# Performance work log

Hardware: AMD Instinct MI355X
Metric: run time of the kernel (lower is better)

Reference implementation:

```python
import jax, jax.numpy as jnp
import numpy as np

NB, H = 4, 16
EPS = 1e-5


def _ln(x, w=None, b=None):
    m = jnp.mean(x, -1, keepdims=True)
    v = jnp.var(x, -1, keepdims=True)
    y = (x - m) * jax.lax.rsqrt(v + EPS)
    if w is not None:
        y = y * w
    if b is not None:
        y = y + b
    return y


def _ada_ln(a, s, ln_s_w, w_gamma, w_beta):
    # AF3 Algorithm 26: a <- sigmoid(Lin(LN_nobias(s))) * LN_noaffine(a) + Lin(LN_nobias(s))
    a_n = _ln(a)
    s_n = _ln(s, ln_s_w)
    return jax.nn.sigmoid(s_n @ w_gamma) * a_n + s_n @ w_beta


def setup_inputs():
    key = jax.random.key(0)
    B, S, c_a, c_s, c_z = 1, 1024, 768, 384, 128
    n_hidden = 2 * c_a  # expansion factor n=2
    ks = iter(jax.random.split(key, 40))

    def rn(shape, scale=1.0):
        return scale * jax.random.normal(next(ks), shape, dtype=jnp.float32)

    p = 0.02
    return {
        "a": rn((B, S, c_a)),
        "s": rn((B, S, c_s)),
        "z": rn((B, S, S, c_z)),
        "beta": rn((B, S, S, H)),
        # per-block AttentionPairBias params (stacked over NB blocks)
        "ln_s_w_attn": jnp.ones((NB, c_s)),
        "wg_attn": rn((NB, c_s, c_a), p),
        "wb_attn": rn((NB, c_s, c_a), p),
        "wq": rn((NB, c_a, c_a), p),
        "bq": jnp.zeros((NB, c_a)),
        "wk": rn((NB, c_a, c_a), p),
        "wv": rn((NB, c_a, c_a), p),
        "ln_z_w": jnp.ones((NB, c_z)),
        "ln_z_b": jnp.zeros((NB, c_z)),
        "wpb": rn((NB, c_z, H), p),
        "wgate": rn((NB, c_a, c_a), p),
        "wo": rn((NB, c_a, c_a), p),
        "wsg_attn": rn((NB, c_s, c_a), p),
        "bsg_attn": -2.0 * jnp.ones((NB, c_a)),
        # per-block ConditionedTransitionBlock params
        "ln_s_w_tr": jnp.ones((NB, c_s)),
        "wg_tr": rn((NB, c_s, c_a), p),
        "wb_tr": rn((NB, c_s, c_a), p),
        "w_swish": rn((NB, c_a, n_hidden), p),
        "w_gate2": rn((NB, c_a, n_hidden), p),
        "wsg_tr": rn((NB, c_s, c_a), p),
        "bsg_tr": -2.0 * jnp.ones((NB, c_a)),
        "w_out": rn((NB, n_hidden, c_a), p),
    }


def reference(a, s, z, beta, ln_s_w_attn, wg_attn, wb_attn, wq, bq, wk, wv,
              ln_z_w, ln_z_b, wpb, wgate, wo, wsg_attn, bsg_attn,
              ln_s_w_tr, wg_tr, wb_tr, w_swish, w_gate2, wsg_tr, bsg_tr, w_out):
    B, S, c_a = a.shape
    d = c_a // H
    scale = 1.0 / jnp.sqrt(jnp.float32(d))
    for i in range(NB):
        # --- AttentionPairBias (AF3 Alg 24) ---
        ah = _ada_ln(a, s, ln_s_w_attn[i], wg_attn[i], wb_attn[i])
        q = (ah @ wq[i] + bq[i]).reshape(B, S, H, d)
        k = (ah @ wk[i]).reshape(B, S, H, d)
        v = (ah @ wv[i]).reshape(B, S, H, d)
        zb = _ln(z, ln_z_w[i], ln_z_b[i]) @ wpb[i]  # [B,S,S,H] pair bias
        scores = jnp.einsum('bihd,bjhd->bhij', q, k) * scale \
                 + jnp.transpose(zb + beta, (0, 3, 1, 2))
        attn = jax.nn.softmax(scores, axis=-1)
        o = jnp.einsum('bhij,bjhd->bihd', attn, v)
        g = jax.nn.sigmoid(ah @ wgate[i]).reshape(B, S, H, d)
        att_out = (g * o).reshape(B, S, c_a) @ wo[i]
        b_attn = jax.nn.sigmoid(s @ wsg_attn[i] + bsg_attn[i]) * att_out
        # --- ConditionedTransitionBlock (AF3 Alg 25, SwiGLU) ---
        th = _ada_ln(a, s, ln_s_w_tr[i], wg_tr[i], wb_tr[i])
        hidden = jax.nn.silu(th @ w_swish[i]) * (th @ w_gate2[i])
        tr = jax.nn.sigmoid(s @ wsg_tr[i] + bsg_tr[i]) * (hidden @ w_out[i])
        a = b_attn + tr
    return a
```

## Files before the change

kernel.cpp:

```cpp
#include <hip/hip_runtime.h>
#include <hip/hip_bf16.h>

typedef __hip_bfloat16 bf16;
typedef __attribute__((ext_vector_type(8))) short s8v;
typedef __attribute__((ext_vector_type(4))) float f4v;

constexpr int S = 1024, CA = 768, CS = 384, CZ = 128, NHID = 1536;
constexpr int NBLK = 4, NHEAD = 16, DH = 48;
constexpr float EPS = 1e-5f;

#define DEV static __device__ __forceinline__

DEV float sigmoidf_(float x) { return 1.0f / (1.0f + __expf(-x)); }

DEV f4v mfma16(s8v a, s8v b, f4v c) {
  return __builtin_amdgcn_mfma_f32_16x16x32_bf16(a, b, c, 0, 0, 0);
}

DEV void gld_lds16(const void* g, void* l) {
  __builtin_amdgcn_global_load_lds((const __attribute__((address_space(1))) void*)g,
                                   (__attribute__((address_space(3))) void*)l, 16, 0, 0);
}

union U8 { s8v s; bf16 h[8]; };
union U4 { uint2 u; bf16 h[4]; };

DEV float wred_sum(float v) {
#pragma unroll
  for (int o = 32; o; o >>= 1) v += __shfl_xor(v, o);
  return v;
}

__global__ __launch_bounds__(256) void rowln_s(const float* __restrict__ x,
                                               bf16* __restrict__ s_hat,
                                               bf16* __restrict__ s_bf) {
  constexpr int C = CS, C4 = C / 4;
  __shared__ float red[8];
  const int t = threadIdx.x;
  const size_t row = blockIdx.x;
  float4 v = make_float4(0.f, 0.f, 0.f, 0.f);
  if (t < C4) v = ((const float4*)(x + row * C))[t];
  float sum = v.x + v.y + v.z + v.w;
  float sq = v.x * v.x + v.y * v.y + v.z * v.z + v.w * v.w;
  sum = wred_sum(sum); sq = wred_sum(sq);
  const int wv = t >> 6;
  if ((t & 63) == 0) { red[2 * wv] = sum; red[2 * wv + 1] = sq; }
  __syncthreads();
  sum = red[0] + red[2] + red[4] + red[6];
  sq = red[1] + red[3] + red[5] + red[7];
  const float m = sum / C;
  const float rstd = rsqrtf(sq / C - m * m + EPS);
  if (t < C4) {
    U4 oh, ob_;
    oh.h[0] = __float2bfloat16((v.x - m) * rstd); oh.h[1] = __float2bfloat16((v.y - m) * rstd);
    oh.h[2] = __float2bfloat16((v.z - m) * rstd); oh.h[3] = __float2bfloat16((v.w - m) * rstd);
    ob_.h[0] = __float2bfloat16(v.x); ob_.h[1] = __float2bfloat16(v.y);
    ob_.h[2] = __float2bfloat16(v.z); ob_.h[3] = __float2bfloat16(v.w);
    *(uint2*)(s_hat + row * C + 4 * t) = oh.u;
    *(uint2*)(s_bf + row * C + 4 * t) = ob_.u;
  }
}

__global__ __launch_bounds__(256) void ln_adaln2(const float* __restrict__ a,
                                                 const bf16* __restrict__ ada,
                                                 bf16* __restrict__ ah_attn,
                                                 bf16* __restrict__ ah_tr) {
  __shared__ float red[8];
  const int t = threadIdx.x;
  const size_t row = blockIdx.x;
  float4 v = make_float4(0.f, 0.f, 0.f, 0.f);
  if (t < 192) v = ((const float4*)(a + row * CA))[t];
  float sum = v.x + v.y + v.z + v.w;
  float sq = v.x * v.x + v.y * v.y + v.z * v.z + v.w * v.w;
  sum = wred_sum(sum); sq = wred_sum(sq);
  const int wv = t >> 6;
  if ((t & 63) == 0) { red[2 * wv] = sum; red[2 * wv + 1] = sq; }
  __syncthreads();
  sum = red[0] + red[2] + red[4] + red[6];
  sq = red[1] + red[3] + red[5] + red[7];
  const float m = sum / CA;
  const float rstd = rsqrtf(sq / CA - m * m + EPS);
  if (t < 192) {
    const float an[4] = {(v.x - m) * rstd, (v.y - m) * rstd, (v.z - m) * rstd, (v.w - m) * rstd};
    const bf16* ar = ada + row * 12288 + 4 * t;
    U4 g1, b1, g2, b2, o1, o2;
    g1.u = *(const uint2*)(ar);
    b1.u = *(const uint2*)(ar + 768);
    g2.u = *(const uint2*)(ar + 1536);
    b2.u = *(const uint2*)(ar + 2304);
#pragma unroll
    for (int j = 0; j < 4; ++j) {
      o1.h[j] = __float2bfloat16(sigmoidf_(__bfloat162float(g1.h[j])) * an[j] + __bfloat162float(b1.h[j]));
      o2.h[j] = __float2bfloat16(sigmoidf_(__bfloat162float(g2.h[j])) * an[j] + __bfloat162float(b2.h[j]));
    }
    *(uint2*)(ah_attn + row * CA + 4 * t) = o1.u;
    *(uint2*)(ah_tr + row * CA + 4 * t) = o2.u;
  }
}

__global__ __launch_bounds__(256) void final_adaln(const float* __restrict__ sg,
                                                   const bf16* __restrict__ att,
                                                   const bf16* __restrict__ tr,
                                                   const bf16* __restrict__ ada,
                                                   bf16* __restrict__ ah_attn,
                                                   bf16* __restrict__ ah_tr) {
  __shared__ float red[8];
  const int t = threadIdx.x;
  const size_t row = blockIdx.x;
  float o[4] = {0.f, 0.f, 0.f, 0.f};
  if (t < 192) {
    const float4 sa = *(const float4*)(sg + row * 6144 + 4 * t);
    const float4 st = *(const float4*)(sg + row * 6144 + 768 + 4 * t);
    U4 av, tv;
    av.u = *(const uint2*)(att + row * CA + 4 * t);
    tv.u = *(const uint2*)(tr + row * CA + 4 * t);
    o[0] = sa.x * __bfloat162float(av.h[0]) + st.x * __bfloat162float(tv.h[0]);
    o[1] = sa.y * __bfloat162float(av.h[1]) + st.y * __bfloat162float(tv.h[1]);
    o[2] = sa.z * __bfloat162float(av.h[2]) + st.z * __bfloat162float(tv.h[2]);
    o[3] = sa.w * __bfloat162float(av.h[3]) + st.w * __bfloat162float(tv.h[3]);
  }
  float sum = o[0] + o[1] + o[2] + o[3];
  float sq = o[0] * o[0] + o[1] * o[1] + o[2] * o[2] + o[3] * o[3];
  sum = wred_sum(sum); sq = wred_sum(sq);
  const int wv = t >> 6;
  if ((t & 63) == 0) { red[2 * wv] = sum; red[2 * wv + 1] = sq; }
  __syncthreads();
  sum = red[0] + red[2] + red[4] + red[6];
  sq = red[1] + red[3] + red[5] + red[7];
  const float m = sum / CA;
  const float rstd = rsqrtf(sq / CA - m * m + EPS);
  if (t < 192) {
    const bf16* ar = ada + row * 12288 + 4 * t;
    U4 g1, b1, g2, b2, o1, o2;
    g1.u = *(const uint2*)(ar);
    b1.u = *(const uint2*)(ar + 768);
    g2.u = *(const uint2*)(ar + 1536);
    b2.u = *(const uint2*)(ar + 2304);
#pragma unroll
    for (int j = 0; j < 4; ++j) {
      const float an = (o[j] - m) * rstd;
      o1.h[j] = __float2bfloat16(sigmoidf_(__bfloat162float(g1.h[j])) * an + __bfloat162float(b1.h[j]));
      o2.h[j] = __float2bfloat16(sigmoidf_(__bfloat162float(g2.h[j])) * an + __bfloat162float(b2.h[j]));
    }
    *(uint2*)(ah_attn + row * CA + 4 * t) = o1.u;
    *(uint2*)(ah_tr + row * CA + 4 * t) = o2.u;
  }
}

struct TGroup {
  const float* src[6];
  bf16* dst[6];
  const float* cs[6];
  long dstZ[6];
};

__global__ __launch_bounds__(256) void transpose_grp(TGroup g, int K, int N, int csZ) {
  __shared__ float tile[32][33];
  const int z = blockIdx.z, wsel = z >> 2, blk = z & 3;
  const float* src = g.src[wsel] + (size_t)blk * K * N;
  bf16* dst = g.dst[wsel] + (size_t)blk * g.dstZ[wsel];
  const float* cs = g.cs[wsel];
  const int k0 = blockIdx.y * 32, n0 = blockIdx.x * 32;
  const int tx = threadIdx.x & 31, ty = threadIdx.x >> 5;
#pragma unroll
  for (int q = 0; q < 4; ++q) {
    const int k = k0 + ty + 8 * q;
    float v = src[(size_t)k * N + n0 + tx];
    if (cs) v *= cs[(size_t)blk * csZ + k];
    tile[ty + 8 * q][tx] = v;
  }
  __syncthreads();
#pragma unroll
  for (int q = 0; q < 4; ++q)
    dst[(size_t)(n0 + ty + 8 * q) * K + k0 + tx] = __float2bfloat16(tile[tx][ty + 8 * q]);
}

__global__ __launch_bounds__(256) void prep_all(const float* __restrict__ ln_z_w,
                                                const float* __restrict__ ln_z_b,
                                                const float* __restrict__ wpb,
                                                bf16* __restrict__ W2T,
                                                float* __restrict__ bias2,
                                                const float* __restrict__ bq,
                                                const float* __restrict__ bsg_attn,
                                                const float* __restrict__ bsg_tr,
                                                float* __restrict__ biasQKVG,
                                                float* __restrict__ biasSG) {
  const int blk = blockIdx.x;
  const int t = threadIdx.x;
  if (blk == 48) {
    for (int f = t; f < 64 * CZ; f += 256) {
      const int col = f >> 7, c = f & 127, b = col >> 4, h = col & 15;
      W2T[f] = __float2bfloat16(ln_z_w[b * CZ + c] * wpb[(b * CZ + c) * NHEAD + h]);
    }
    if (t < 64) {
      const int b = t >> 4, h = t & 15;
      float sum = 0.f;
      for (int c = 0; c < CZ; ++c)
        sum += ln_z_b[b * CZ + c] * wpb[(b * CZ + c) * NHEAD + h];
      bias2[t] = sum;
    }
    return;
  }
  const int g = blk * 256 + t;
  if (g < 4 * 3072) {
    const int b = g / 3072, c = g % 3072;
    biasQKVG[g] = (c < 768) ? bq[b * 768 + c] : 0.f;
  }
  if (g < 6144) {
    const int b = g / 1536, c = g % 1536;
    biasSG[g] = (c < 768) ? bsg_attn[b * 768 + c] : bsg_tr[b * 768 + c - 768];
  }
}

__global__ __launch_bounds__(256) void zbias_kernel(const float* __restrict__ z,
                                                    const float* __restrict__ beta,
                                                    const bf16* __restrict__ W2T,
                                                    const float* __restrict__ bias2,
                                                    bf16* __restrict__ bias_all) {
  __shared__ s8v zt8[64 * 16];
  __shared__ s8v w2s[64 * 16];
  __shared__ float betas[64][17];
  __shared__ float bias2s[64];
  __shared__ bf16 obuf[64][72];
  const int t = threadIdx.x;
  const int i = blockIdx.y, j0 = blockIdx.x * 64;
#pragma unroll
  for (int q = 0; q < 4; ++q) {
    const int u = q * 256 + t;
    const int row = u >> 4, sl = u & 15;
    w2s[row * 16 + (sl ^ (row & 7))] = *(const s8v*)(W2T + row * CZ + sl * 8);
  }
  if (t < 64) bias2s[t] = bias2[t];
  {
    const int j = t >> 2, h4 = t & 3;
    const float4 bv = *(const float4*)(beta + ((size_t)i * S + j0 + j) * NHEAD + 4 * h4);
    betas[j][4 * h4 + 0] = bv.x; betas[j][4 * h4 + 1] = bv.y;
    betas[j][4 * h4 + 2] = bv.z; betas[j][4 * h4 + 3] = bv.w;
  }
  {
    const int p = t >> 2, q = t & 3;
    const float* zr = z + ((size_t)i * S + j0 + p) * CZ + q * 32;
    float vals[32];
    float sum = 0.f, sq = 0.f;
#pragma unroll
    for (int k4 = 0; k4 < 8; ++k4) {
      const float4 xv = *(const float4*)(zr + 4 * k4);
      vals[4 * k4 + 0] = xv.x; vals[4 * k4 + 1] = xv.y;
      vals[4 * k4 + 2] = xv.z; vals[4 * k4 + 3] = xv.w;
      sum += xv.x + xv.y + xv.z + xv.w;
      sq += xv.x * xv.x + xv.y * xv.y + xv.z * xv.z + xv.w * xv.w;
    }
    sum += __shfl_xor(sum, 1); sum += __shfl_xor(sum, 2);
    sq += __shfl_xor(sq, 1); sq += __shfl_xor(sq, 2);
    const float m = sum / CZ;
    const float rstd = rsqrtf(sq / CZ - m * m + EPS);
#pragma unroll
    for (int u = 0; u < 4; ++u) {
      U8 pk;
#pragma unroll
      for (int e = 0; e < 8; ++e) pk.h[e] = __float2bfloat16((vals[8 * u + e] - m) * rstd);
      const int cu = 4 * q + u;
      zt8[p * 16 + (cu ^ (p & 7))] = pk.s;
    }
  }
  __syncthreads();
  const int lane = t & 63, wid = t >> 6;
  const int wr = wid >> 1, wc = wid & 1;
  const int ln = lane & 15, lq = lane >> 4;
  f4v acc[2][2] = {};
#pragma unroll
  for (int kk = 0; kk < 4; ++kk) {
    const int sl = (lq + 4 * kk) ^ (ln & 7);
    s8v a[2], b[2];
#pragma unroll
    for (int mi = 0; mi < 2; ++mi) a[mi] = zt8[(32 * wr + 16 * mi + ln) * 16 + sl];
#pragma unroll
    for (int ni = 0; ni < 2; ++ni) b[ni] = w2s[(32 * wc + 16 * ni + ln) * 16 + sl];
#pragma unroll
    for (int mi = 0; mi < 2; ++mi)
#pragma unroll
      for (int ni = 0; ni < 2; ++ni) acc[mi][ni] = mfma16(a[mi], b[ni], acc[mi][ni]);
  }
#pragma unroll
  for (int mi = 0; mi < 2; ++mi)
#pragma unroll
    for (int ni = 0; ni < 2; ++ni) {
      const int col = 32 * wc + 16 * ni + ln;
      const int jb = 32 * wr + 16 * mi + 4 * lq;
      U4 o4;
#pragma unroll
      for (int r = 0; r < 4; ++r)
        o4.h[r] = __float2bfloat16(acc[mi][ni][r] + bias2s[col] + betas[jb + r][col & 15]);
      *(uint2*)&obuf[col][jb] = o4.u;
    }
  __syncthreads();
  {
    const int oc = t >> 2, js = (t & 3) * 16;
    bf16* dp = bias_all + (size_t)oc * S * S + (size_t)i * S + j0 + js;
    *(s8v*)dp = *(const s8v*)&obuf[oc][js];
    *(s8v*)(dp + 8) = *(const s8v*)&obuf[oc][js + 8];
  }
}

struct Gemm2Args {
  const bf16* A0[2]; int lda0[2];
  const bf16* Bt[2];
  const float* bias[2];
  void* C[2];
  int K[2];
  int nb[2];
  int outMode[2];
  int N[2];
  bf16* vT;
};

__global__ __launch_bounds__(256) void gemm2(Gemm2Args ga) {
  const int z = blockIdx.z;
  if ((int)blockIdx.x >= ga.nb[z]) return;
  __shared__ s8v As[1024];
  __shared__ s8v Bs[1024];
  const bf16* A0 = ga.A0[z]; const int lda0 = ga.lda0[z];
  const bf16* Bt = ga.Bt[z];
  const int K = ga.K[z], N = ga.N[z];
  const int t = threadIdx.x;
  const int lane = t & 63, wid = t >> 6;
  const int wr = wid >> 1, wc = wid & 1;
  const int ln = lane & 15, lq = lane >> 4;
  const int m0 = blockIdx.y * 128, n0 = blockIdx.x * 128;
  int rowA[4], colx[4];
#pragma unroll
  for (int q = 0; q < 4; ++q) {
    const int u = q * 256 + t, row = u >> 3, slp = u & 7;
    rowA[q] = row; colx[q] = (slp ^ (row & 7)) * 8;
  }
  f4v acc[4][4] = {};
  for (int ks = 0; ks < K; ks += 64) {
    __syncthreads();
#pragma unroll
    for (int q = 0; q < 4; ++q) {
      gld_lds16(A0 + (size_t)(m0 + rowA[q]) * lda0 + ks + colx[q], &As[q * 256 + wid * 64]);
      gld_lds16(Bt + (size_t)(n0 + rowA[q]) * K + ks + colx[q], &Bs[q * 256 + wid * 64]);
    }
    __syncthreads();
#pragma unroll
    for (int kk = 0; kk < 2; ++kk) {
      const int sl = (lq + 4 * kk) ^ (ln & 7);
      s8v a[4], b[4];
#pragma unroll
      for (int mi = 0; mi < 4; ++mi) a[mi] = As[(64 * wr + 16 * mi + ln) * 8 + sl];
#pragma unroll
      for (int ni = 0; ni < 4; ++ni) b[ni] = Bs[(64 * wc + 16 * ni + ln) * 8 + sl];
#pragma unroll
      for (int mi = 0; mi < 4; ++mi)
#pragma unroll
        for (int ni = 0; ni < 4; ++ni) acc[mi][ni] = mfma16(a[mi], b[ni], acc[mi][ni]);
    }
  }
  const bool vdiv = (ga.vT != nullptr) && (z == 0) && (n0 >= 1536) && (n0 < 2304);
  const int om = ga.outMode[z];
#pragma unroll
  for (int ni = 0; ni < 4; ++ni) {
    const int n = n0 + 64 * wc + 16 * ni + ln;
    const float bv = ga.bias[z] ? ga.bias[z][n] : 0.f;
#pragma unroll
    for (int mi = 0; mi < 4; ++mi) {
      const int mb = m0 + 64 * wr + 16 * mi + 4 * lq;
      if (vdiv) {
        U4 o4;
#pragma unroll
        for (int r = 0; r < 4; ++r) o4.h[r] = __float2bfloat16(acc[mi][ni][r] + bv);
        *(uint2*)(ga.vT + (size_t)(n - 1536) * S + mb) = o4.u;
      } else if (om == 0) {
        bf16* C = (bf16*)ga.C[z];
#pragma unroll
        for (int r = 0; r < 4; ++r)
          C[(size_t)(mb + r) * N + n] = __float2bfloat16(acc[mi][ni][r] + bv);
      } else {
        float* C = (float*)ga.C[z];
#pragma unroll
        for (int r = 0; r < 4; ++r)
          C[(size_t)(mb + r) * N + n] = sigmoidf_(acc[mi][ni][r] + bv);
      }
    }
  }
}

struct GemmPairArgs {
  const bf16* A0[2]; int lda0[2];
  const bf16* A1[2]; int lda1[2];
  const bf16* Bt[2];
  const float* bias[2];
  bf16* C[2];
  int K[2]; int amode[2];
};

DEV s8v combineRT(s8v x, s8v y, int amode) {
  U8 ux, uy, r;
  ux.s = x; uy.s = y;
#pragma unroll
  for (int j = 0; j < 8; ++j) {
    const float fx = __bfloat162float(ux.h[j]);
    const float fy = __bfloat162float(uy.h[j]);
    const float tt = sigmoidf_(fx);
    r.h[j] = __float2bfloat16((amode == 2 ? fx * tt : tt) * fy);
  }
  return r.s;
}

__global__ __launch_bounds__(256) void gemm_pair(GemmPairArgs ga, int N) {
  __shared__ s8v As[128 * 8];
  __shared__ s8v Bs[128 * 8];
  const int z = blockIdx.z;
  const bf16* A0 = ga.A0[z]; const int lda0 = ga.lda0[z];
  const bf16* A1 = ga.A1[z]; const int lda1 = ga.lda1[z];
  const bf16* Bt = ga.Bt[z];
  const float* bias = ga.bias[z];
  bf16* C = ga.C[z];
  const int K = ga.K[z], amode = ga.amode[z];
  const int t = threadIdx.x;
  const int lane = t & 63, wid = t >> 6;
  const int wr = wid >> 1, wc = wid & 1;
  const int ln = lane & 15, lq = lane >> 4;
  const int m0 = blockIdx.y * 128, n0 = blockIdx.x * 128;
  int rowS[4], slS[4], swz[4];
#pragma unroll
  for (int q = 0; q < 4; ++q) {
    const int u = q * 256 + t;
    rowS[q] = u >> 3; slS[q] = u & 7;
    swz[q] = rowS[q] * 8 + (slS[q] ^ (rowS[q] & 7));
  }
  f4v acc[4][4] = {};
  s8v ra[4], ra2[4], rb[4];
#pragma unroll
  for (int q = 0; q < 4; ++q) {
    ra[q] = *(const s8v*)(A0 + (size_t)(m0 + rowS[q]) * lda0 + slS[q] * 8);
    if (amode != 0) ra2[q] = *(const s8v*)(A1 + (size_t)(m0 + rowS[q]) * lda1 + slS[q] * 8);
    rb[q] = *(const s8v*)(Bt + (size_t)(n0 + rowS[q]) * K + slS[q] * 8);
  }
  for (int ks = 0;;) {
    __syncthreads();
#pragma unroll
    for (int q = 0; q < 4; ++q) {
      As[swz[q]] = (amode == 0) ? ra[q] : combineRT(ra[q], ra2[q], amode);
      Bs[swz[q]] = rb[q];
    }
    const int ksn = ks + 64;
    if (ksn < K) {
#pragma unroll
      for (int q = 0; q < 4; ++q) {
        ra[q] = *(const s8v*)(A0 + (size_t)(m0 + rowS[q]) * lda0 + ksn + slS[q] * 8);
        if (amode != 0) ra2[q] = *(const s8v*)(A1 + (size_t)(m0 + rowS[q]) * lda1 + ksn + slS[q] * 8);
        rb[q] = *(const s8v*)(Bt + (size_t)(n0 + rowS[q]) * K + ksn + slS[q] * 8);
      }
    }
    __syncthreads();
#pragma unroll
    for (int kk = 0; kk < 2; ++kk) {
      const int sl = (lq + 4 * kk) ^ (ln & 7);
      s8v a[4], b[4];
#pragma unroll
      for (int mi = 0; mi < 4; ++mi) a[mi] = As[(64 * wr + 16 * mi + ln) * 8 + sl];
#pragma unroll
      for (int ni = 0; ni < 4; ++ni) b[ni] = Bs[(64 * wc + 16 * ni + ln) * 8 + sl];
#pragma unroll
      for (int mi = 0; mi < 4; ++mi)
#pragma unroll
        for (int ni = 0; ni < 4; ++ni) acc[mi][ni] = mfma16(a[mi], b[ni], acc[mi][ni]);
    }
    ks = ksn;
    if (ks >= K) break;
  }
#pragma unroll
  for (int ni = 0; ni < 4; ++ni) {
    const int n = n0 + 64 * wc + 16 * ni + ln;
    const float bv = bias ? bias[n] : 0.f;
#pragma unroll
    for (int mi = 0; mi < 4; ++mi) {
      const int mb = m0 + 64 * wr + 16 * mi + 4 * lq;
#pragma unroll
      for (int r = 0; r < 4; ++r)
        C[(size_t)(mb + r) * N + n] = __float2bfloat16(acc[mi][ni][r] + bv);
    }
  }
}

__global__ __launch_bounds__(256) void flash_attn(const bf16* __restrict__ qkvg,
                                                  const bf16* __restrict__ vT,
                                                  const bf16* __restrict__ bias_all,
                                                  bf16* __restrict__ ob, int blk) {
  __shared__ s8v Qs[64 * 8];
  __shared__ s8v Ks[2][64 * 8];
  __shared__ s8v Vs[2][48 * 8];
  __shared__ s8v Bs[2][64 * 8];
  __shared__ bf16 PwB[4 * 1024];
  __shared__ float facL[4][16];
  __shared__ float linvL[4][16];
  const int t = threadIdx.x;
  const int lane = t & 63, w = t >> 6;
  const int ln = lane & 15, lq = lane >> 4;
  const int h = blockIdx.y, i0 = blockIdx.x * 64;
  const bf16* bp = bias_all + (size_t)(blk * NHEAD + h) * S * S;
  const float scale = 0.14433756729740643f;

#pragma unroll
  for (int uu = 0; uu < 2; ++uu) {
    const int u = t + 256 * uu, row = u >> 3, sl = u & 7;
    s8v qv{};
    if (sl < 6) qv = *(const s8v*)(qkvg + (size_t)(i0 + row) * 3072 + h * DH + sl * 8);
    Qs[row * 8 + (sl ^ (row & 7))] = qv;
  }

  s8v kr[2], br[2], vr0{}, vr1{};
  auto prefetch = [&](int jt) {
    const int j0 = jt * 64;
#pragma unroll
    for (int uu = 0; uu < 2; ++uu) {
      const int u = t + 256 * uu, row = u >> 3, sl = u & 7;
      s8v kv{};
      if (sl < 6) kv = *(const s8v*)(qkvg + (size_t)(j0 + row) * 3072 + 768 + h * DH + sl * 8);
      kr[uu] = kv;
      br[uu] = *(const s8v*)(bp + (size_t)(i0 + row) * S + j0 + sl * 8);
    }
    { const int d = t >> 3, sl = t & 7;
      vr0 = *(const s8v*)(vT + (size_t)(h * DH + d) * S + j0 + sl * 8); }
    if (t < 128) {
      const int u = 256 + t, d = u >> 3, sl = u & 7;
      vr1 = *(const s8v*)(vT + (size_t)(h * DH + d) * S + j0 + sl * 8);
    }
  };
  auto store_tiles = [&](int pb) {
#pragma unroll
    for (int uu = 0; uu < 2; ++uu) {
      const int u = t + 256 * uu, row = u >> 3, sl = u & 7;
      const int ph = row * 8 + (sl ^ (row & 7));
      Ks[pb][ph] = kr[uu];
      Bs[pb][ph] = br[uu];
    }
    { const int d = t >> 3, sl = t & 7;
      Vs[pb][d * 8 + (sl ^ (d & 7))] = vr0; }
    if (t < 128) {
      const int u = 256 + t, d = u >> 3, sl = u & 7;
      Vs[pb][d * 8 + (sl ^ (d & 7))] = vr1;
    }
  };

  float m_run = -3e30f, l_run = 0.f;
  f4v acc_o[3] = {};
  bf16* pw = PwB + w * 1024;

  prefetch(0);
  for (int jt = 0; jt < 16; ++jt) {
    const int pb = jt & 1;
    __syncthreads();
    store_tiles(pb);
    __syncthreads();
    if (jt < 15) prefetch(jt + 1);
    float p[4][4];
    float tmax = -3e30f;
#pragma unroll
    for (int ja = 0; ja < 4; ++ja) {
      f4v accs = {};
#pragma unroll
      for (int ks2 = 0; ks2 < 2; ++ks2) {
        const int sl = (lq + 4 * ks2) ^ (ln & 7);
        const s8v a = Ks[pb][(16 * ja + ln) * 8 + sl];
        const s8v b = Qs[(16 * w + ln) * 8 + sl];
        accs = mfma16(a, b, accs);
      }
      const int jq = 4 * ja + lq;
      const int pu = jq >> 1;
      U4 bv;
      bv.u = *(const uint2*)((const bf16*)(&Bs[pb][0]) +
                             (((16 * w + ln) * 8 + (pu ^ (ln & 7))) * 8 + (jq & 1) * 4));
#pragma unroll
      for (int r = 0; r < 4; ++r) {
        p[ja][r] = accs[r] * scale + __bfloat162float(bv.h[r]);
        tmax = fmaxf(tmax, p[ja][r]);
      }
    }
    tmax = fmaxf(tmax, __shfl_xor(tmax, 16));
    tmax = fmaxf(tmax, __shfl_xor(tmax, 32));
    const float m_new = fmaxf(m_run, tmax);
    const float fac = __expf(m_run - m_new);
    m_run = m_new;
    float psum = 0.f;
#pragma unroll
    for (int ja = 0; ja < 4; ++ja)
#pragma unroll
      for (int r = 0; r < 4; ++r) {
        p[ja][r] = __expf(p[ja][r] - m_new);
        psum += p[ja][r];
      }
    psum += __shfl_xor(psum, 16);
    psum += __shfl_xor(psum, 32);
    l_run = l_run * fac + psum;
    if (lq == 0) facL[w][ln] = fac;
#pragma unroll
    for (int ja = 0; ja < 4; ++ja) {
      const int ju = 4 * ja + lq;
      const int ph = ju ^ ((ln & 7) << 1);
      U4 pk;
#pragma unroll
      for (int r = 0; r < 4; ++r) pk.h[r] = __float2bfloat16(p[ja][r]);
      *(uint2*)(pw + ln * 64 + ph * 4) = pk.u;
    }
    asm volatile("s_waitcnt lgkmcnt(0)" ::: "memory");
    __builtin_amdgcn_sched_barrier(0);
    const float4 fv = *(const float4*)&facL[w][4 * lq];
#pragma unroll
    for (int ni = 0; ni < 3; ++ni) {
      acc_o[ni][0] *= fv.x; acc_o[ni][1] *= fv.y;
      acc_o[ni][2] *= fv.z; acc_o[ni][3] *= fv.w;
    }
#pragma unroll
    for (int ks2 = 0; ks2 < 2; ++ks2) {
      const int pu0 = (2 * lq + 8 * ks2) ^ ((ln & 7) << 1);
      const s8v pa = *(const s8v*)(pw + ln * 64 + pu0 * 4);
      const int slv = (lq + 4 * ks2) ^ (ln & 7);
#pragma unroll
      for (int ni = 0; ni < 3; ++ni) {
        const s8v vb = Vs[pb][(16 * ni + ln) * 8 + slv];
        acc_o[ni] = mfma16(pa, vb, acc_o[ni]);
      }
    }
  }
  if (lq == 0) linvL[w][ln] = 1.0f / l_run;
  asm volatile("s_waitcnt lgkmcnt(0)" ::: "memory");
  __builtin_amdgcn_sched_barrier(0);
  const float4 lv = *(const float4*)&linvL[w][4 * lq];
  const float lvr[4] = {lv.x, lv.y, lv.z, lv.w};
#pragma unroll
  for (int ni = 0; ni < 3; ++ni)
#pragma unroll
    for (int r = 0; r < 4; ++r) {
      const int m = i0 + 16 * w + 4 * lq + r;
      ob[(size_t)m * CA + h * DH + 16 * ni + ln] = __float2bfloat16(acc_o[ni][r] * lvr[r]);
    }
}

__global__ __launch_bounds__(256) void ew_final(const float* __restrict__ sg,
                                                const bf16* __restrict__ att,
                                                const bf16* __restrict__ tr,
                                                float* __restrict__ out) {
  const int i = blockIdx.x * 256 + threadIdx.x;
  const int row = i / 192, col = (i % 192) * 4;
  const float4 sa = *(const float4*)(sg + (size_t)row * 6144 + col);
  const float4 st = *(const float4*)(sg + (size_t)row * 6144 + 768 + col);
  U4 av, tv;
  av.u = *(const uint2*)(att + (size_t)row * CA + col);
  tv.u = *(const uint2*)(tr + (size_t)row * CA + col);
  float4 o;
  o.x = sa.x * __bfloat162float(av.h[0]) + st.x * __bfloat162float(tv.h[0]);
  o.y = sa.y * __bfloat162float(av.h[1]) + st.y * __bfloat162float(tv.h[1]);
  o.z = sa.z * __bfloat162float(av.h[2]) + st.z * __bfloat162float(tv.h[2]);
  o.w = sa.w * __bfloat162float(av.h[3]) + st.w * __bfloat162float(tv.h[3]);
  *(float4*)(out + (size_t)row * CA + col) = o;
}

__global__ void fill_kernel(float* p, int n, float v) {
  const int i = blockIdx.x * 256 + threadIdx.x;
  if (i < n) p[i] = v;
}

extern "C" void kernel_launch(void* const* d_in, const int* in_sizes, int n_in,
                              void* d_out, int out_size, void* d_ws, size_t ws_size,
                              hipStream_t stream) {
  (void)in_sizes; (void)n_in;
  const float* a_in = (const float*)d_in[0];
  const float* s_in = (const float*)d_in[1];
  const float* z_in = (const float*)d_in[2];
  const float* beta = (const float*)d_in[3];
  const float* ln_s_w_attn = (const float*)d_in[4];
  const float* wg_attn = (const float*)d_in[5];
  const float* wb_attn = (const float*)d_in[6];
  const float* wq = (const float*)d_in[7];
  const float* bq = (const float*)d_in[8];
  const float* wk = (const float*)d_in[9];
  const float* wv = (const float*)d_in[10];
  const float* ln_z_w = (const float*)d_in[11];
  const float* ln_z_b = (const float*)d_in[12];
  const float* wpb = (const float*)d_in[13];
  const float* wgate = (const float*)d_in[14];
  const float* wo = (const float*)d_in[15];
  const float* wsg_attn = (const float*)d_in[16];
  const float* bsg_attn = (const float*)d_in[17];
  const float* ln_s_w_tr = (const float*)d_in[18];
  const float* wg_tr = (const float*)d_in[19];
  const float* wb_tr = (const float*)d_in[20];
  const float* w_swish = (const float*)d_in[21];
  const float* w_gate2 = (const float*)d_in[22];
  const float* wsg_tr = (const float*)d_in[23];
  const float* bsg_tr = (const float*)d_in[24];
  const float* w_out = (const float*)d_in[25];

  char* wp = (char*)d_ws;
  size_t used = 0;
  auto alloc = [&](size_t bytes) -> void* {
    void* p = wp + used;
    used += (bytes + 255) & ~(size_t)255;
    return p;
  };
  bf16* bias_all = (bf16*)alloc((size_t)64 * S * S * 2);
  bf16* WT_ada = (bf16*)alloc((size_t)4 * 3072 * 384 * 2);
  bf16* WT_sg = (bf16*)alloc((size_t)4 * 1536 * 384 * 2);
  bf16* WT_qkvg = (bf16*)alloc((size_t)4 * 3072 * 768 * 2);
  bf16* WT_wo = (bf16*)alloc((size_t)4 * 768 * 768 * 2);
  bf16* WT_mlp = (bf16*)alloc((size_t)4 * 3072 * 768 * 2);
  bf16* WT_wout = (bf16*)alloc((size_t)4 * 768 * 1536 * 2);
  float* biasQKVG = (float*)alloc(4 * 3072 * 4);
  float* biasSG = (float*)alloc(6144 * 4);
  bf16* W2T = (bf16*)alloc(64 * 128 * 2);
  float* bias2 = (float*)alloc(64 * 4);
  bf16* ada_all = (bf16*)alloc((size_t)S * 12288 * 2);
  float* sg_all = (float*)alloc((size_t)S * 6144 * 4);
  bf16* s_hat = (bf16*)alloc((size_t)S * CS * 2);
  bf16* s_bf = (bf16*)alloc((size_t)S * CS * 2);
  bf16* ah_attn = (bf16*)alloc((size_t)S * CA * 2);
  bf16* ah_tr = (bf16*)alloc((size_t)S * CA * 2);
  bf16* qkvg = (bf16*)alloc((size_t)S * 3072 * 2);
  bf16* vT = (bf16*)alloc((size_t)CA * S * 2);
  bf16* ob = (bf16*)alloc((size_t)S * CA * 2);
  bf16* att = (bf16*)alloc((size_t)S * CA * 2);
  bf16* swg = (bf16*)alloc((size_t)S * 3072 * 2);
  bf16* trout = (bf16*)alloc((size_t)S * CA * 2);
  if (used > ws_size) {
    fill_kernel<<<(out_size + 255) / 256, 256, 0, stream>>>((float*)d_out, out_size, 12345.0f);
    return;
  }

  const dim3 B256(256);

  prep_all<<<49, B256, 0, stream>>>(ln_z_w, ln_z_b, wpb, W2T, bias2,
                                    bq, bsg_attn, bsg_tr, biasQKVG, biasSG);

  {
    TGroup g{};
    g.src[0] = wg_attn;  g.dst[0] = WT_ada + (size_t)0 * 384;    g.cs[0] = ln_s_w_attn; g.dstZ[0] = 3072 * 384;
    g.src[1] = wb_attn;  g.dst[1] = WT_ada + (size_t)768 * 384;  g.cs[1] = ln_s_w_attn; g.dstZ[1] = 3072 * 384;
    g.src[2] = wg_tr;    g.dst[2] = WT_ada + (size_t)1536 * 384; g.cs[2] = ln_s_w_tr;   g.dstZ[2] = 3072 * 384;
    g.src[3] = wb_tr;    g.dst[3] = WT_ada + (size_t)2304 * 384; g.cs[3] = ln_s_w_tr;   g.dstZ[3] = 3072 * 384;
    g.src[4] = wsg_attn; g.dst[4] = WT_sg + (size_t)0 * 384;     g.cs[4] = nullptr;     g.dstZ[4] = 1536 * 384;
    g.src[5] = wsg_tr;   g.dst[5] = WT_sg + (size_t)768 * 384;   g.cs[5] = nullptr;     g.dstZ[5] = 1536 * 384;
    transpose_grp<<<dim3(24, 12, 24), B256, 0, stream>>>(g, 384, 768, CS);
  }
  {
    TGroup g{};
    g.src[0] = wq;    g.dst[0] = WT_qkvg + (size_t)0 * 768;    g.dstZ[0] = 3072 * 768;
    g.src[1] = wk;    g.dst[1] = WT_qkvg + (size_t)768 * 768;  g.dstZ[1] = 3072 * 768;
    g.src[2] = wv;    g.dst[2] = WT_qkvg + (size_t)1536 * 768; g.dstZ[2] = 3072 * 768;
    g.src[3] = wgate; g.dst[3] = WT_qkvg + (size_t)2304 * 768; g.dstZ[3] = 3072 * 768;
    g.src[4] = wo;    g.dst[4] = WT_wo;                        g.dstZ[4] = 768 * 768;
    transpose_grp<<<dim3(24, 24, 20), B256, 0, stream>>>(g, 768, 768, 0);
  }
  {
    TGroup g{};
    g.src[0] = w_swish; g.dst[0] = WT_mlp + (size_t)0 * 768;    g.dstZ[0] = 3072 * 768;
    g.src[1] = w_gate2; g.dst[1] = WT_mlp + (size_t)1536 * 768; g.dstZ[1] = 3072 * 768;
    transpose_grp<<<dim3(48, 24, 8), B256, 0, stream>>>(g, 768, 1536, 0);
  }
  {
    TGroup g{};
    g.src[0] = w_out; g.dst[0] = WT_wout; g.dstZ[0] = 768 * 1536;
    transpose_grp<<<dim3(24, 48, 4), B256, 0, stream>>>(g, 1536, 768, 0);
  }

  rowln_s<<<S, B256, 0, stream>>>(s_in, s_hat, s_bf);
  zbias_kernel<<<dim3(16, 1024), B256, 0, stream>>>(z_in, beta, W2T, bias2, bias_all);

  {
    Gemm2Args ga{};
    ga.A0[0] = s_hat; ga.lda0[0] = 384; ga.Bt[0] = WT_ada; ga.bias[0] = nullptr;
    ga.C[0] = ada_all; ga.K[0] = 384; ga.nb[0] = 96; ga.outMode[0] = 0; ga.N[0] = 12288;
    ga.A0[1] = s_bf; ga.lda0[1] = 384; ga.Bt[1] = WT_sg; ga.bias[1] = biasSG;
    ga.C[1] = sg_all; ga.K[1] = 384; ga.nb[1] = 48; ga.outMode[1] = 1; ga.N[1] = 6144;
    ga.vT = nullptr;
    gemm2<<<dim3(96, 8, 2), B256, 0, stream>>>(ga);
  }

  ln_adaln2<<<S, B256, 0, stream>>>(a_in, ada_all, ah_attn, ah_tr);
  for (int b = 0; b < NBLK; ++b) {
    {
      Gemm2Args ga{};
      ga.A0[0] = ah_attn; ga.lda0[0] = 768; ga.Bt[0] = WT_qkvg + (size_t)b * 3072 * 768;
      ga.bias[0] = biasQKVG + b * 3072; ga.C[0] = qkvg; ga.K[0] = 768; ga.nb[0] = 24;
      ga.outMode[0] = 0; ga.N[0] = 3072;
      ga.A0[1] = ah_tr; ga.lda0[1] = 768; ga.Bt[1] = WT_mlp + (size_t)b * 3072 * 768;
      ga.bias[1] = nullptr; ga.C[1] = swg; ga.K[1] = 768; ga.nb[1] = 24;
      ga.outMode[1] = 0; ga.N[1] = 3072;
      ga.vT = vT;
      gemm2<<<dim3(24, 8, 2), B256, 0, stream>>>(ga);
    }
    flash_attn<<<dim3(16, 16), B256, 0, stream>>>(qkvg, vT, bias_all, ob, b);
    {
      GemmPairArgs ga{};
      ga.A0[0] = qkvg + 2304; ga.lda0[0] = 3072; ga.A1[0] = ob; ga.lda1[0] = 768;
      ga.Bt[0] = WT_wo + (size_t)b * 768 * 768; ga.bias[0] = nullptr;
      ga.C[0] = att; ga.K[0] = 768; ga.amode[0] = 1;
      ga.A0[1] = swg; ga.lda0[1] = 3072; ga.A1[1] = swg + 1536; ga.lda1[1] = 3072;
      ga.Bt[1] = WT_wout + (size_t)b * 768 * 1536; ga.bias[1] = nullptr;
      ga.C[1] = trout; ga.K[1] = 1536; ga.amode[1] = 2;
      gemm_pair<<<dim3(6, 8, 2), B256, 0, stream>>>(ga, 768);
    }
    if (b < NBLK - 1) {
      final_adaln<<<S, B256, 0, stream>>>(sg_all + (size_t)b * 1536, att, trout,
                                          ada_all + (size_t)(b + 1) * 3072, ah_attn, ah_tr);
    } else {
      ew_final<<<768, B256, 0, stream>>>(sg_all + (size_t)b * 1536, att, trout, (float*)d_out);
    }
  }
}
```

Before: 676.6 us.

## Merge prep kernels and co-schedule independent work in fat kernels

Collapses the weight transposes, bias prep and s layernorm into one launch, and runs the z pair-bias kernel alongside the adaLN/gate GEMMs in a single interleaved grid. Inside each block, attention runs in the same launch as the transition output GEMM, and the Wo GEMM moves to its own kernel. The aim is fewer launches and idle tails by overlapping independent work. The cost is heterogeneous blocks with larger shared memory per block, which may lower occupancy.

```diff
diff --git a/kernel.cpp b/kernel.cpp
--- a/kernel.cpp
+++ b/kernel.cpp
@@ -31,34 +31,561 @@
   return v;
 }
 
-__global__ __launch_bounds__(256) void rowln_s(const float* __restrict__ x,
-                                               bf16* __restrict__ s_hat,
-                                               bf16* __restrict__ s_bf) {
-  constexpr int C = CS, C4 = C / 4;
-  __shared__ float red[8];
-  const int t = threadIdx.x;
-  const size_t row = blockIdx.x;
-  float4 v = make_float4(0.f, 0.f, 0.f, 0.f);
-  if (t < C4) v = ((const float4*)(x + row * C))[t];
-  float sum = v.x + v.y + v.z + v.w;
-  float sq = v.x * v.x + v.y * v.y + v.z * v.z + v.w * v.w;
-  sum = wred_sum(sum); sq = wred_sum(sq);
-  const int wv = t >> 6;
-  if ((t & 63) == 0) { red[2 * wv] = sum; red[2 * wv + 1] = sq; }
+struct PrepFatArgs {
+  const float* tsrc[14];
+  bf16* tdst[14];
+  const float* tcs[14];
+  long tdstZ[14];
+  const float *ln_z_w, *ln_z_b, *wpb, *bq, *bsg_a, *bsg_t;
+  bf16* W2T; float* bias2; float* biasQKVG; float* biasSG;
+  const float* s_in; bf16* s_hat; bf16* s_bf;
+};
+
+__global__ __launch_bounds__(256) void prep_fat(PrepFatArgs a) {
+  __shared__ __align__(16) float tile[1056];
+  const int bid = blockIdx.x, t = threadIdx.x;
+  if (bid < 32256) {
+    int ti, blk, x, y, K, N;
+    if (bid < 6912) {
+      const int lb = bid; ti = lb / 1152; const int r2 = lb % 1152;
+      blk = r2 / 288; const int rem = r2 % 288; x = rem % 24; y = rem / 24; K = 384; N = 768;
+    } else if (bid < 18432) {
+      const int lb = bid - 6912; ti = 6 + lb / 2304; const int r2 = lb % 2304;
+      blk = r2 / 576; const int rem = r2 % 576; x = rem % 24; y = rem / 24; K = 768; N = 768;
+    } else if (bid < 27648) {
+      const int lb = bid - 18432; ti = 11 + lb / 4608; const int r2 = lb % 4608;
+      blk = r2 / 1152; const int rem = r2 % 1152; x = rem % 48; y = rem / 48; K = 768; N = 1536;
+    } else {
+      const int lb = bid - 27648; ti = 13; blk = lb / 1152;
+      const int rem = lb % 1152; x = rem % 24; y = rem / 24; K = 1536; N = 768;
+    }
+    const float* src = a.tsrc[ti] + (size_t)blk * K * N;
+    bf16* dst = a.tdst[ti] + (size_t)blk * a.tdstZ[ti];
+    const float* cs = a.tcs[ti] ? (a.tcs[ti] + blk * CS) : nullptr;
+    const int k0 = y * 32, n0 = x * 32, tx = t & 31, ty = t >> 5;
+#pragma unroll
+    for (int q = 0; q < 4; ++q) {
+      const int k = k0 + ty + 8 * q;
+      float v = src[(size_t)k * N + n0 + tx];
+      if (cs) v *= cs[k];
+      tile[(ty + 8 * q) * 33 + tx] = v;
+    }
+    __syncthreads();
+#pragma unroll
+    for (int q = 0; q < 4; ++q)
+      dst[(size_t)(n0 + ty + 8 * q) * K + k0 + tx] = __float2bfloat16(tile[tx * 33 + ty + 8 * q]);
+    return;
+  }
+  if (bid < 32305) {
+    const int pid = bid - 32256;
+    if (pid == 48) {
+      for (int f = t; f < 64 * CZ; f += 256) {
+        const int col = f >> 7, c = f & 127, b = col >> 4, h = col & 15;
+        a.W2T[f] = __float2bfloat16(a.ln_z_w[b * CZ + c] * a.wpb[(b * CZ + c) * NHEAD + h]);
+      }
+      if (t < 64) {
+        const int b = t >> 4, h = t & 15;
+        float sum = 0.f;
+        for (int c = 0; c < CZ; ++c)
+          sum += a.ln_z_b[b * CZ + c] * a.wpb[(b * CZ + c) * NHEAD + h];
+        a.bias2[t] = sum;
+      }
+      return;
+    }
+    const int g = pid * 256 + t;
+    if (g < 4 * 3072) {
+      const int b = g / 3072, c = g % 3072;
+      a.biasQKVG[g] = (c < 768) ? a.bq[b * 768 + c] : 0.f;
+    }
+    if (g < 6144) {
+      const int b = g / 1536, c = g % 1536;
+      a.biasSG[g] = (c < 768) ? a.bsg_a[b * 768 + c] : a.bsg_t[b * 768 + c - 768];
+    }
+    return;
+  }
+  {
+    float* red = tile;
+    const size_t row = bid - 32305;
+    float4 v = make_float4(0.f, 0.f, 0.f, 0.f);
+    if (t < CS / 4) v = ((const float4*)(a.s_in + row * CS))[t];
+    float sum = v.x + v.y + v.z + v.w;
+    float sq = v.x * v.x + v.y * v.y + v.z * v.z + v.w * v.w;
+    sum = wred_sum(sum); sq = wred_sum(sq);
+    const int wv = t >> 6;
+    if ((t & 63) == 0) { red[2 * wv] = sum; red[2 * wv + 1] = sq; }
+    __syncthreads();
+    sum = red[0] + red[2] + red[4] + red[6];
+    sq = red[1] + red[3] + red[5] + red[7];
+    const float m = sum / CS;
+    const float rstd = rsqrtf(sq / CS - m * m + EPS);
+    if (t < CS / 4) {
+      U4 oh, ob_;
+      oh.h[0] = __float2bfloat16((v.x - m) * rstd); oh.h[1] = __float2bfloat16((v.y - m) * rstd);
+      oh.h[2] = __float2bfloat16((v.z - m) * rstd); oh.h[3] = __float2bfloat16((v.w - m) * rstd);
+      ob_.h[0] = __float2bfloat16(v.x); ob_.h[1] = __float2bfloat16(v.y);
+      ob_.h[2] = __float2bfloat16(v.z); ob_.h[3] = __float2bfloat16(v.w);
+      *(uint2*)(a.s_hat + row * CS + 4 * t) = oh.u;
+      *(uint2*)(a.s_bf + row * CS + 4 * t) = ob_.u;
+    }
+  }
+}
+
+DEV void zbias_core(char* smem, const float* __restrict__ z, const float* __restrict__ beta,
+                    const bf16* __restrict__ W2T, const float* __restrict__ bias2,
+                    bf16* __restrict__ bias_all, int jt, int i, int t) {
+  s8v* zt8 = (s8v*)smem;
+  s8v* w2s = (s8v*)(smem + 16384);
+  float* betas = (float*)(smem + 32768);
+  float* bias2s = (float*)(smem + 37120);
+  bf16* obuf = (bf16*)(smem + 37376);
+  const int j0 = jt * 64;
+#pragma unroll
+  for (int q = 0; q < 4; ++q) {
+    const int u = q * 256 + t;
+    const int row = u >> 4, sl = u & 15;
+    w2s[row * 16 + (sl ^ (row & 7))] = *(const s8v*)(W2T + row * CZ + sl * 8);
+  }
+  if (t < 64) bias2s[t] = bias2[t];
+  {
+    const int j = t >> 2, h4 = t & 3;
+    const float4 bv = *(const float4*)(beta + ((size_t)i * S + j0 + j) * NHEAD + 4 * h4);
+    betas[j * 17 + 4 * h4 + 0] = bv.x; betas[j * 17 + 4 * h4 + 1] = bv.y;
+    betas[j * 17 + 4 * h4 + 2] = bv.z; betas[j * 17 + 4 * h4 + 3] = bv.w;
+  }
+  {
+    const int p = t >> 2, q = t & 3;
+    const float* zr = z + ((size_t)i * S + j0 + p) * CZ + q * 32;
+    float vals[32];
+    float sum = 0.f, sq = 0.f;
+#pragma unroll
+    for (int k4 = 0; k4 < 8; ++k4) {
+      const float4 xv = *(const float4*)(zr + 4 * k4);
+      vals[4 * k4 + 0] = xv.x; vals[4 * k4 + 1] = xv.y;
+      vals[4 * k4 + 2] = xv.z; vals[4 * k4 + 3] = xv.w;
+      sum += xv.x + xv.y + xv.z + xv.w;
+      sq += xv.x * xv.x + xv.y * xv.y + xv.z * xv.z + xv.w * xv.w;
+    }
+    sum += __shfl_xor(sum, 1); sum += __shfl_xor(sum, 2);
+    sq += __shfl_xor(sq, 1); sq += __shfl_xor(sq, 2);
+    const float m = sum / CZ;
+    const float rstd = rsqrtf(sq / CZ - m * m + EPS);
+#pragma unroll
+    for (int u = 0; u < 4; ++u) {
+      U8 pk;
+#pragma unroll
+      for (int e = 0; e < 8; ++e) pk.h[e] = __float2bfloat16((vals[8 * u + e] - m) * rstd);
+      const int cu = 4 * q + u;
+      zt8[p * 16 + (cu ^ (p & 7))] = pk.s;
+    }
+  }
   __syncthreads();
-  sum = red[0] + red[2] + red[4] + red[6];
-  sq = red[1] + red[3] + red[5] + red[7];
-  const float m = sum / C;
-  const float rstd = rsqrtf(sq / C - m * m + EPS);
-  if (t < C4) {
-    U4 oh, ob_;
-    oh.h[0] = __float2bfloat16((v.x - m) * rstd); oh.h[1] = __float2bfloat16((v.y - m) * rstd);
-    oh.h[2] = __float2bfloat16((v.z - m) * rstd); oh.h[3] = __float2bfloat16((v.w - m) * rstd);
-    ob_.h[0] = __float2bfloat16(v.x); ob_.h[1] = __float2bfloat16(v.y);
-    ob_.h[2] = __float2bfloat16(v.z); ob_.h[3] = __float2bfloat16(v.w);
-    *(uint2*)(s_hat + row * C + 4 * t) = oh.u;
-    *(uint2*)(s_bf + row * C + 4 * t) = ob_.u;
-  }
+  const int lane = t & 63, wid = t >> 6;
+  const int wr = wid >> 1, wc = wid & 1;
+  const int ln = lane & 15, lq = lane >> 4;
+  f4v acc[2][2] = {};
+#pragma unroll
+  for (int kk = 0; kk < 4; ++kk) {
+    const int sl = (lq + 4 * kk) ^ (ln & 7);
+    s8v aa[2], bb[2];
+#pragma unroll
+    for (int mi = 0; mi < 2; ++mi) aa[mi] = zt8[(32 * wr + 16 * mi + ln) * 16 + sl];
+#pragma unroll
+    for (int ni = 0; ni < 2; ++ni) bb[ni] = w2s[(32 * wc + 16 * ni + ln) * 16 + sl];
+#pragma unroll
+    for (int mi = 0; mi < 2; ++mi)
+#pragma unroll
+      for (int ni = 0; ni < 2; ++ni) acc[mi][ni] = mfma16(aa[mi], bb[ni], acc[mi][ni]);
+  }
+#pragma unroll
+  for (int mi = 0; mi < 2; ++mi)
+#pragma unroll
+    for (int ni = 0; ni < 2; ++ni) {
+      const int col = 32 * wc + 16 * ni + ln;
+      const int jb = 32 * wr + 16 * mi + 4 * lq;
+      U4 o4;
+#pragma unroll
+      for (int r = 0; r < 4; ++r)
+        o4.h[r] = __float2bfloat16(acc[mi][ni][r] + bias2s[col] + betas[(jb + r) * 17 + (col & 15)]);
+      *(uint2*)&obuf[col * 72 + jb] = o4.u;
+    }
+  __syncthreads();
+  {
+    const int oc = t >> 2, js = (t & 3) * 16;
+    bf16* dp = bias_all + (size_t)oc * S * S + (size_t)i * S + j0 + js;
+    *(s8v*)dp = *(const s8v*)&obuf[oc * 72 + js];
+    *(s8v*)(dp + 8) = *(const s8v*)&obuf[oc * 72 + js + 8];
+  }
+}
+
+DEV void gemm2_core(char* smem, const bf16* __restrict__ A0, int lda0,
+                    const bf16* __restrict__ Bt, const float* __restrict__ bias,
+                    void* C, int K, int N, int outMode, bf16* vT, bool vdiv,
+                    int m0, int n0, int t) {
+  s8v* As = (s8v*)smem;
+  s8v* Bs = (s8v*)(smem + 16384);
+  const int lane = t & 63, wid = t >> 6;
+  const int wr = wid >> 1, wc = wid & 1;
+  const int ln = lane & 15, lq = lane >> 4;
+  int rowA[4], colx[4];
+#pragma unroll
+  for (int q = 0; q < 4; ++q) {
+    const int u = q * 256 + t, row = u >> 3, slp = u & 7;
+    rowA[q] = row; colx[q] = (slp ^ (row & 7)) * 8;
+  }
+  f4v acc[4][4] = {};
+  for (int ks = 0; ks < K; ks += 64) {
+    __syncthreads();
+#pragma unroll
+    for (int q = 0; q < 4; ++q) {
+      gld_lds16(A0 + (size_t)(m0 + rowA[q]) * lda0 + ks + colx[q], &As[q * 256 + wid * 64]);
+      gld_lds16(Bt + (size_t)(n0 + rowA[q]) * K + ks + colx[q], &Bs[q * 256 + wid * 64]);
+    }
+    __syncthreads();
+#pragma unroll
+    for (int kk = 0; kk < 2; ++kk) {
+      const int sl = (lq + 4 * kk) ^ (ln & 7);
+      s8v a[4], b[4];
+#pragma unroll
+      for (int mi = 0; mi < 4; ++mi) a[mi] = As[(64 * wr + 16 * mi + ln) * 8 + sl];
+#pragma unroll
+      for (int ni = 0; ni < 4; ++ni) b[ni] = Bs[(64 * wc + 16 * ni + ln) * 8 + sl];
+#pragma unroll
+      for (int mi = 0; mi < 4; ++mi)
+#pragma unroll
+        for (int ni = 0; ni < 4; ++ni) acc[mi][ni] = mfma16(a[mi], b[ni], acc[mi][ni]);
+    }
+  }
+#pragma unroll
+  for (int ni = 0; ni < 4; ++ni) {
+    const int n = n0 + 64 * wc + 16 * ni + ln;
+    const float bv = bias ? bias[n] : 0.f;
+#pragma unroll
+    for (int mi = 0; mi < 4; ++mi) {
+      const int mb = m0 + 64 * wr + 16 * mi + 4 * lq;
+      if (vdiv) {
+        U4 o4;
+#pragma unroll
+        for (int r = 0; r < 4; ++r) o4.h[r] = __float2bfloat16(acc[mi][ni][r] + bv);
+        *(uint2*)(vT + (size_t)(n - 1536) * S + mb) = o4.u;
+      } else if (outMode == 0) {
+        bf16* Cb = (bf16*)C;
+#pragma unroll
+        for (int r = 0; r < 4; ++r)
+          Cb[(size_t)(mb + r) * N + n] = __float2bfloat16(acc[mi][ni][r] + bv);
+      } else {
+        float* Cf = (float*)C;
+#pragma unroll
+        for (int r = 0; r < 4; ++r)
+          Cf[(size_t)(mb + r) * N + n] = sigmoidf_(acc[mi][ni][r] + bv);
+      }
+    }
+  }
+}
+
+struct Mega1Args {
+  const float* z; const float* beta; const bf16* W2T; const float* bias2; bf16* bias_all;
+  const bf16* s_hat; const bf16* s_bf; const bf16* WT_ada; const bf16* WT_sg;
+  const float* biasSG; bf16* ada_all; float* sg_all;
+};
+
+__global__ __launch_bounds__(256) void mega1(Mega1Args a) {
+  __shared__ __align__(16) char smem[46592];
+  const int bid = blockIdx.x, t = threadIdx.x;
+  const int q = bid / 15, r = bid % 15;
+  if (r == 7 && q < 1152) {
+    if (q < 768) {
+      gemm2_core(smem, a.s_hat, 384, a.WT_ada, nullptr, a.ada_all, 384, 12288, 0,
+                 nullptr, false, (q / 96) * 128, (q % 96) * 128, t);
+    } else {
+      const int qq = q - 768;
+      gemm2_core(smem, a.s_bf, 384, a.WT_sg, a.biasSG, a.sg_all, 384, 6144, 1,
+                 nullptr, false, (qq / 48) * 128, (qq % 48) * 128, t);
+    }
+    return;
+  }
+  const int idx = bid - ((q < 1152 ? q : 1152) + ((r > 7 && q < 1152) ? 1 : 0));
+  zbias_core(smem, a.z, a.beta, a.W2T, a.bias2, a.bias_all, idx & 15, idx >> 4, t);
+}
+
+struct Gemm2Args {
+  const bf16* A0[2]; int lda0[2];
+  const bf16* Bt[2];
+  const float* bias[2];
+  void* C[2];
+  int K[2]; int N[2];
+  bf16* vT;
+};
+
+__global__ __launch_bounds__(256) void gemm2(Gemm2Args ga) {
+  __shared__ __align__(16) char smem[32768];
+  const int z = blockIdx.z;
+  const int m0 = blockIdx.y * 128, n0 = blockIdx.x * 128;
+  const bool vdiv = (ga.vT != nullptr) && (z == 0) && (n0 >= 1536) && (n0 < 2304);
+  gemm2_core(smem, ga.A0[z], ga.lda0[z], ga.Bt[z], ga.bias[z], ga.C[z], ga.K[z], ga.N[z],
+             0, ga.vT, vdiv, m0, n0, threadIdx.x);
+}
+
+DEV s8v combineRT(s8v x, s8v y, int amode) {
+  U8 ux, uy, rr;
+  ux.s = x; uy.s = y;
+#pragma unroll
+  for (int j = 0; j < 8; ++j) {
+    const float fx = __bfloat162float(ux.h[j]);
+    const float fy = __bfloat162float(uy.h[j]);
+    const float tt = sigmoidf_(fx);
+    rr.h[j] = __float2bfloat16((amode == 2 ? fx * tt : tt) * fy);
+  }
+  return rr.s;
+}
+
+DEV void gemm_combA_core(char* smem, const bf16* __restrict__ A0, int lda0,
+                         const bf16* __restrict__ A1, int lda1,
+                         const bf16* __restrict__ Bt, const float* __restrict__ bias,
+                         bf16* __restrict__ C, int K, int N, int amode,
+                         int m0, int n0, int t) {
+  s8v* As = (s8v*)smem;
+  s8v* Bs = (s8v*)(smem + 16384);
+  const int lane = t & 63, wid = t >> 6;
+  const int wr = wid >> 1, wc = wid & 1;
+  const int ln = lane & 15, lq = lane >> 4;
+  int rowS[4], slS[4], swz[4];
+#pragma unroll
+  for (int q = 0; q < 4; ++q) {
+    const int u = q * 256 + t;
+    rowS[q] = u >> 3; slS[q] = u & 7;
+    swz[q] = rowS[q] * 8 + (slS[q] ^ (rowS[q] & 7));
+  }
+  f4v acc[4][4] = {};
+  s8v ra[4], ra2[4], rb[4];
+#pragma unroll
+  for (int q = 0; q < 4; ++q) {
+    ra[q] = *(const s8v*)(A0 + (size_t)(m0 + rowS[q]) * lda0 + slS[q] * 8);
+    ra2[q] = *(const s8v*)(A1 + (size_t)(m0 + rowS[q]) * lda1 + slS[q] * 8);
+    rb[q] = *(const s8v*)(Bt + (size_t)(n0 + rowS[q]) * K + slS[q] * 8);
+  }
+  for (int ks = 0;;) {
+    __syncthreads();
+#pragma unroll
+    for (int q = 0; q < 4; ++q) {
+      As[swz[q]] = combineRT(ra[q], ra2[q], amode);
+      Bs[swz[q]] = rb[q];
+    }
+    const int ksn = ks + 64;
+    if (ksn < K) {
+#pragma unroll
+      for (int q = 0; q < 4; ++q) {
+        ra[q] = *(const s8v*)(A0 + (size_t)(m0 + rowS[q]) * lda0 + ksn + slS[q] * 8);
+        ra2[q] = *(const s8v*)(A1 + (size_t)(m0 + rowS[q]) * lda1 + ksn + slS[q] * 8);
+        rb[q] = *(const s8v*)(Bt + (size_t)(n0 + rowS[q]) * K + ksn + slS[q] * 8);
+      }
+    }
+    __syncthreads();
+#pragma unroll
+    for (int kk = 0; kk < 2; ++kk) {
+      const int sl = (lq + 4 * kk) ^ (ln & 7);
+      s8v a[4], b[4];
+#pragma unroll
+      for (int mi = 0; mi < 4; ++mi) a[mi] = As[(64 * wr + 16 * mi + ln) * 8 + sl];
+#pragma unroll
+      for (int ni = 0; ni < 4; ++ni) b[ni] = Bs[(64 * wc + 16 * ni + ln) * 8 + sl];
+#pragma unroll
+      for (int mi = 0; mi < 4; ++mi)
+#pragma unroll
+        for (int ni = 0; ni < 4; ++ni) acc[mi][ni] = mfma16(a[mi], b[ni], acc[mi][ni]);
+    }
+    ks = ksn;
+    if (ks >= K) break;
+  }
+#pragma unroll
+  for (int ni = 0; ni < 4; ++ni) {
+    const int n = n0 + 64 * wc + 16 * ni + ln;
+    const float bv = bias ? bias[n] : 0.f;
+#pragma unroll
+    for (int mi = 0; mi < 4; ++mi) {
+      const int mb = m0 + 64 * wr + 16 * mi + 4 * lq;
+#pragma unroll
+      for (int r = 0; r < 4; ++r)
+        C[(size_t)(mb + r) * N + n] = __float2bfloat16(acc[mi][ni][r] + bv);
+    }
+  }
+}
+
+DEV void flash_core(char* smem, const bf16* __restrict__ qkvg, const bf16* __restrict__ vT,
+                    const bf16* __restrict__ bp, bf16* __restrict__ ob, int itile, int h, int t) {
+  s8v* Qs = (s8v*)smem;
+  s8v* KsB = (s8v*)(smem + 8192);
+  s8v* VsB = (s8v*)(smem + 24576);
+  s8v* BsB = (s8v*)(smem + 36864);
+  bf16* PwB = (bf16*)(smem + 53248);
+  float* facL = (float*)(smem + 61440);
+  float* linvL = (float*)(smem + 61696);
+  const int lane = t & 63, w = t >> 6;
+  const int ln = lane & 15, lq = lane >> 4;
+  const int i0 = itile * 64;
+  const float scale = 0.14433756729740643f;
+
+#pragma unroll
+  for (int uu = 0; uu < 2; ++uu) {
+    const int u = t + 256 * uu, row = u >> 3, sl = u & 7;
+    s8v qv{};
+    if (sl < 6) qv = *(const s8v*)(qkvg + (size_t)(i0 + row) * 3072 + h * DH + sl * 8);
+    Qs[row * 8 + (sl ^ (row & 7))] = qv;
+  }
+
+  s8v kr[2], br[2], vr0{}, vr1{};
+  auto prefetch = [&](int jt) {
+    const int j0 = jt * 64;
+#pragma unroll
+    for (int uu = 0; uu < 2; ++uu) {
+      const int u = t + 256 * uu, row = u >> 3, sl = u & 7;
+      s8v kv{};
+      if (sl < 6) kv = *(const s8v*)(qkvg + (size_t)(j0 + row) * 3072 + 768 + h * DH + sl * 8);
+      kr[uu] = kv;
+      br[uu] = *(const s8v*)(bp + (size_t)(i0 + row) * S + j0 + sl * 8);
+    }
+    { const int d = t >> 3, sl = t & 7;
+      vr0 = *(const s8v*)(vT + (size_t)(h * DH + d) * S + j0 + sl * 8); }
+    if (t < 128) {
+      const int u = 256 + t, d = u >> 3, sl = u & 7;
+      vr1 = *(const s8v*)(vT + (size_t)(h * DH + d) * S + j0 + sl * 8);
+    }
+  };
+  auto store_tiles = [&](int pb) {
+#pragma unroll
+    for (int uu = 0; uu < 2; ++uu) {
+      const int u = t + 256 * uu, row = u >> 3, sl = u & 7;
+      const int ph = row * 8 + (sl ^ (row & 7));
+      KsB[pb * 512 + ph] = kr[uu];
+      BsB[pb * 512 + ph] = br[uu];
+    }
+    { const int d = t >> 3, sl = t & 7;
+      VsB[pb * 384 + d * 8 + (sl ^ (d & 7))] = vr0; }
+    if (t < 128) {
+      const int u = 256 + t, d = u >> 3, sl = u & 7;
+      VsB[pb * 384 + d * 8 + (sl ^ (d & 7))] = vr1;
+    }
+  };
+
+  float m_run = -3e30f, l_run = 0.f;
+  f4v acc_o[3] = {};
+  bf16* pw = PwB + w * 1024;
+
+  prefetch(0);
+  for (int jt = 0; jt < 16; ++jt) {
+    const int pb = jt & 1;
+    __syncthreads();
+    store_tiles(pb);
+    __syncthreads();
+    if (jt < 15) prefetch(jt + 1);
+    float p[4][4];
+    float tmax = -3e30f;
+#pragma unroll
+    for (int ja = 0; ja < 4; ++ja) {
+      f4v accs = {};
+#pragma unroll
+      for (int ks2 = 0; ks2 < 2; ++ks2) {
+        const int sl = (lq + 4 * ks2) ^ (ln & 7);
+        const s8v a = KsB[pb * 512 + (16 * ja + ln) * 8 + sl];
+        const s8v b = Qs[(16 * w + ln) * 8 + sl];
+        accs = mfma16(a, b, accs);
+      }
+      const int jq = 4 * ja + lq;
+      const int pu = jq >> 1;
+      U4 bv;
+      bv.u = *(const uint2*)((const bf16*)(BsB + pb * 512) +
+                             (((16 * w + ln) * 8 + (pu ^ (ln & 7))) * 8 + (jq & 1) * 4));
+#pragma unroll
+      for (int r = 0; r < 4; ++r) {
+        p[ja][r] = accs[r] * scale + __bfloat162float(bv.h[r]);
+        tmax = fmaxf(tmax, p[ja][r]);
+      }
+    }
+    tmax = fmaxf(tmax, __shfl_xor(tmax, 16));
+    tmax = fmaxf(tmax, __shfl_xor(tmax, 32));
+    const float m_new = fmaxf(m_run, tmax);
+    const float fac = __expf(m_run - m_new);
+    m_run = m_new;
+    float psum = 0.f;
+#pragma unroll
+    for (int ja = 0; ja < 4; ++ja)
+#pragma unroll
+      for (int r = 0; r < 4; ++r) {
+        p[ja][r] = __expf(p[ja][r] - m_new);
+        psum += p[ja][r];
+      }
+    psum += __shfl_xor(psum, 16);
+    psum += __shfl_xor(psum, 32);
+    l_run = l_run * fac + psum;
+    if (lq == 0) facL[w * 16 + ln] = fac;
+#pragma unroll
+    for (int ja = 0; ja < 4; ++ja) {
+      const int ju = 4 * ja + lq;
+      const int ph = ju ^ ((ln & 7) << 1);
+      U4 pk;
+#pragma unroll
+      for (int r = 0; r < 4; ++r) pk.h[r] = __float2bfloat16(p[ja][r]);
+      *(uint2*)(pw + ln * 64 + ph * 4) = pk.u;
+    }
+    asm volatile("s_waitcnt lgkmcnt(0)" ::: "memory");
+    __builtin_amdgcn_sched_barrier(0);
+    const float4 fv = *(const float4*)&facL[w * 16 + 4 * lq];
+#pragma unroll
+    for (int ni = 0; ni < 3; ++ni) {
+      acc_o[ni][0] *= fv.x; acc_o[ni][1] *= fv.y;
+      acc_o[ni][2] *= fv.z; acc_o[ni][3] *= fv.w;
+    }
+#pragma unroll
+    for (int ks2 = 0; ks2 < 2; ++ks2) {
+      const int pu0 = (2 * lq + 8 * ks2) ^ ((ln & 7) << 1);
+      const s8v pa = *(const s8v*)(pw + ln * 64 + pu0 * 4);
+      const int slv = (lq + 4 * ks2) ^ (ln & 7);
+#pragma unroll
+      for (int ni = 0; ni < 3; ++ni) {
+        const s8v vb = VsB[pb * 384 + (16 * ni + ln) * 8 + slv];
+        acc_o[ni] = mfma16(pa, vb, acc_o[ni]);
+      }
+    }
+  }
+  if (lq == 0) linvL[w * 16 + ln] = 1.0f / l_run;
+  asm volatile("s_waitcnt lgkmcnt(0)" ::: "memory");
+  __builtin_amdgcn_sched_barrier(0);
+  const float4 lv = *(const float4*)&linvL[w * 16 + 4 * lq];
+  const float lvr[4] = {lv.x, lv.y, lv.z, lv.w};
+#pragma unroll
+  for (int ni = 0; ni < 3; ++ni)
+#pragma unroll
+    for (int r = 0; r < 4; ++r) {
+      const int m = i0 + 16 * w + 4 * lq + r;
+      ob[(size_t)m * CA + h * DH + 16 * ni + ln] = __float2bfloat16(acc_o[ni][r] * lvr[r]);
+    }
+}
+
+struct FlashFatArgs {
+  const bf16* qkvg; const bf16* vT; const bf16* bias_b; bf16* ob;
+  const bf16* swg; const bf16* WT_wout_b; bf16* trout;
+};
+
+__global__ __launch_bounds__(256) void flash_fat(FlashFatArgs a) {
+  __shared__ __align__(16) char smem[61952];
+  const int bid = blockIdx.x, t = threadIdx.x;
+  const int q = bid / 6, r = bid % 6;
+  if (r == 3 && q < 48) {
+    gemm_combA_core(smem, a.swg, 3072, a.swg + 1536, 3072, a.WT_wout_b, nullptr,
+                    a.trout, 1536, 768, 2, (q / 6) * 128, (q % 6) * 128, t);
+    return;
+  }
+  const int idx = bid - ((q < 48 ? q : 48) + ((r > 3 && q < 48) ? 1 : 0));
+  flash_core(smem, a.qkvg, a.vT, a.bias_b + (size_t)(idx >> 4) * S * S, a.ob,
+             idx & 15, idx >> 4, t);
+}
+
+__global__ __launch_bounds__(256) void gemm_wo(const bf16* __restrict__ gate,
+                                               const bf16* __restrict__ ob,
+                                               const bf16* __restrict__ Bt,
+                                               bf16* __restrict__ C) {
+  __shared__ __align__(16) char smem[32768];
+  gemm_combA_core(smem, gate, 3072, ob, 768, Bt, nullptr, C, 768, 768, 1,
+                  blockIdx.y * 128, blockIdx.x * 128, threadIdx.x);
 }
 
 __global__ __launch_bounds__(256) void ln_adaln2(const float* __restrict__ a,
@@ -145,497 +672,6 @@
     *(uint2*)(ah_attn + row * CA + 4 * t) = o1.u;
     *(uint2*)(ah_tr + row * CA + 4 * t) = o2.u;
   }
-}
-
-struct TGroup {
-  const float* src[6];
-  bf16* dst[6];
-  const float* cs[6];
-  long dstZ[6];
-};
-
-__global__ __launch_bounds__(256) void transpose_grp(TGroup g, int K, int N, int csZ) {
-  __shared__ float tile[32][33];
-  const int z = blockIdx.z, wsel = z >> 2, blk = z & 3;
-  const float* src = g.src[wsel] + (size_t)blk * K * N;
-  bf16* dst = g.dst[wsel] + (size_t)blk * g.dstZ[wsel];
-  const float* cs = g.cs[wsel];
-  const int k0 = blockIdx.y * 32, n0 = blockIdx.x * 32;
-  const int tx = threadIdx.x & 31, ty = threadIdx.x >> 5;
-#pragma unroll
-  for (int q = 0; q < 4; ++q) {
-    const int k = k0 + ty + 8 * q;
-    float v = src[(size_t)k * N + n0 + tx];
-    if (cs) v *= cs[(size_t)blk * csZ + k];
-    tile[ty + 8 * q][tx] = v;
-  }
-  __syncthreads();
-#pragma unroll
-  for (int q = 0; q < 4; ++q)
-    dst[(size_t)(n0 + ty + 8 * q) * K + k0 + tx] = __float2bfloat16(tile[tx][ty + 8 * q]);
-}
-
-__global__ __launch_bounds__(256) void prep_all(const float* __restrict__ ln_z_w,
-                                                const float* __restrict__ ln_z_b,
-                                                const float* __restrict__ wpb,
-                                                bf16* __restrict__ W2T,
-                                                float* __restrict__ bias2,
-                                                const float* __restrict__ bq,
-                                                const float* __restrict__ bsg_attn,
-                                                const float* __restrict__ bsg_tr,
-                                                float* __restrict__ biasQKVG,
-                                                float* __restrict__ biasSG) {
-  const int blk = blockIdx.x;
-  const int t = threadIdx.x;
-  if (blk == 48) {
-    for (int f = t; f < 64 * CZ; f += 256) {
-      const int col = f >> 7, c = f & 127, b = col >> 4, h = col & 15;
-      W2T[f] = __float2bfloat16(ln_z_w[b * CZ + c] * wpb[(b * CZ + c) * NHEAD + h]);
-    }
-    if (t < 64) {
-      const int b = t >> 4, h = t & 15;
-      float sum = 0.f;
-      for (int c = 0; c < CZ; ++c)
-        sum += ln_z_b[b * CZ + c] * wpb[(b * CZ + c) * NHEAD + h];
-      bias2[t] = sum;
-    }
-    return;
-  }
-  const int g = blk * 256 + t;
-  if (g < 4 * 3072) {
-    const int b = g / 3072, c = g % 3072;
-    biasQKVG[g] = (c < 768) ? bq[b * 768 + c] : 0.f;
-  }
-  if (g < 6144) {
-    const int b = g / 1536, c = g % 1536;
-    biasSG[g] = (c < 768) ? bsg_attn[b * 768 + c] : bsg_tr[b * 768 + c - 768];
-  }
-}
-
-__global__ __launch_bounds__(256) void zbias_kernel(const float* __restrict__ z,
-                                                    const float* __restrict__ beta,
-                                                    const bf16* __restrict__ W2T,
-                                                    const float* __restrict__ bias2,
-                                                    bf16* __restrict__ bias_all) {
-  __shared__ s8v zt8[64 * 16];
-  __shared__ s8v w2s[64 * 16];
-  __shared__ float betas[64][17];
-  __shared__ float bias2s[64];
-  __shared__ bf16 obuf[64][72];
-  const int t = threadIdx.x;
-  const int i = blockIdx.y, j0 = blockIdx.x * 64;
-#pragma unroll
-  for (int q = 0; q < 4; ++q) {
-    const int u = q * 256 + t;
-    const int row = u >> 4, sl = u & 15;
-    w2s[row * 16 + (sl ^ (row & 7))] = *(const s8v*)(W2T + row * CZ + sl * 8);
-  }
-  if (t < 64) bias2s[t] = bias2[t];
-  {
-    const int j = t >> 2, h4 = t & 3;
-    const float4 bv = *(const float4*)(beta + ((size_t)i * S + j0 + j) * NHEAD + 4 * h4);
-    betas[j][4 * h4 + 0] = bv.x; betas[j][4 * h4 + 1] = bv.y;
-    betas[j][4 * h4 + 2] = bv.z; betas[j][4 * h4 + 3] = bv.w;
-  }
-  {
-    const int p = t >> 2, q = t & 3;
-    const float* zr = z + ((size_t)i * S + j0 + p) * CZ + q * 32;
-    float vals[32];
-    float sum = 0.f, sq = 0.f;
-#pragma unroll
-    for (int k4 = 0; k4 < 8; ++k4) {
-      const float4 xv = *(const float4*)(zr + 4 * k4);
-      vals[4 * k4 + 0] = xv.x; vals[4 * k4 + 1] = xv.y;
-      vals[4 * k4 + 2] = xv.z; vals[4 * k4 + 3] = xv.w;
-      sum += xv.x + xv.y + xv.z + xv.w;
-      sq += xv.x * xv.x + xv.y * xv.y + xv.z * xv.z + xv.w * xv.w;
-    }
-    sum += __shfl_xor(sum, 1); sum += __shfl_xor(sum, 2);
-    sq += __shfl_xor(sq, 1); sq += __shfl_xor(sq, 2);
-    const float m = sum / CZ;
-    const float rstd = rsqrtf(sq / CZ - m * m + EPS);
-#pragma unroll
-    for (int u = 0; u < 4; ++u) {
-      U8 pk;
-#pragma unroll
-      for (int e = 0; e < 8; ++e) pk.h[e] = __float2bfloat16((vals[8 * u + e] - m) * rstd);
-      const int cu = 4 * q + u;
-      zt8[p * 16 + (cu ^ (p & 7))] = pk.s;
-    }
-  }
-  __syncthreads();
-  const int lane = t & 63, wid = t >> 6;
-  const int wr = wid >> 1, wc = wid & 1;
-  const int ln = lane & 15, lq = lane >> 4;
-  f4v acc[2][2] = {};
-#pragma unroll
-  for (int kk = 0; kk < 4; ++kk) {
-    const int sl = (lq + 4 * kk) ^ (ln & 7);
-    s8v a[2], b[2];
-#pragma unroll
-    for (int mi = 0; mi < 2; ++mi) a[mi] = zt8[(32 * wr + 16 * mi + ln) * 16 + sl];
-#pragma unroll
-    for (int ni = 0; ni < 2; ++ni) b[ni] = w2s[(32 * wc + 16 * ni + ln) * 16 + sl];
-#pragma unroll
-    for (int mi = 0; mi < 2; ++mi)
-#pragma unroll
-      for (int ni = 0; ni < 2; ++ni) acc[mi][ni] = mfma16(a[mi], b[ni], acc[mi][ni]);
-  }
-#pragma unroll
-  for (int mi = 0; mi < 2; ++mi)
-#pragma unroll
-    for (int ni = 0; ni < 2; ++ni) {
-      const int col = 32 * wc + 16 * ni + ln;
-      const int jb = 32 * wr + 16 * mi + 4 * lq;
-      U4 o4;
-#pragma unroll
-      for (int r = 0; r < 4; ++r)
-        o4.h[r] = __float2bfloat16(acc[mi][ni][r] + bias2s[col] + betas[jb + r][col & 15]);
-      *(uint2*)&obuf[col][jb] = o4.u;
-    }
-  __syncthreads();
-  {
-    const int oc = t >> 2, js = (t & 3) * 16;
-    bf16* dp = bias_all + (size_t)oc * S * S + (size_t)i * S + j0 + js;
-    *(s8v*)dp = *(const s8v*)&obuf[oc][js];
-    *(s8v*)(dp + 8) = *(const s8v*)&obuf[oc][js + 8];
-  }
-}
-
-struct Gemm2Args {
-  const bf16* A0[2]; int lda0[2];
-  const bf16* Bt[2];
-  const float* bias[2];
-  void* C[2];
-  int K[2];
-  int nb[2];
-  int outMode[2];
-  int N[2];
-  bf16* vT;
-};
-
-__global__ __launch_bounds__(256) void gemm2(Gemm2Args ga) {
-  const int z = blockIdx.z;
-  if ((int)blockIdx.x >= ga.nb[z]) return;
-  __shared__ s8v As[1024];
-  __shared__ s8v Bs[1024];
-  const bf16* A0 = ga.A0[z]; const int lda0 = ga.lda0[z];
-  const bf16* Bt = ga.Bt[z];
-  const int K = ga.K[z], N = ga.N[z];
-  const int t = threadIdx.x;
-  const int lane = t & 63, wid = t >> 6;
-  const int wr = wid >> 1, wc = wid & 1;
-  const int ln = lane & 15, lq = lane >> 4;
-  const int m0 = blockIdx.y * 128, n0 = blockIdx.x * 128;
-  int rowA[4], colx[4];
-#pragma unroll
-  for (int q = 0; q < 4; ++q) {
-    const int u = q * 256 + t, row = u >> 3, slp = u & 7;
-    rowA[q] = row; colx[q] = (slp ^ (row & 7)) * 8;
-  }
-  f4v acc[4][4] = {};
-  for (int ks = 0; ks < K; ks += 64) {
-    __syncthreads();
-#pragma unroll
-    for (int q = 0; q < 4; ++q) {
-      gld_lds16(A0 + (size_t)(m0 + rowA[q]) * lda0 + ks + colx[q], &As[q * 256 + wid * 64]);
-      gld_lds16(Bt + (size_t)(n0 + rowA[q]) * K + ks + colx[q], &Bs[q * 256 + wid * 64]);
-    }
-    __syncthreads();
-#pragma unroll
-    for (int kk = 0; kk < 2; ++kk) {
-      const int sl = (lq + 4 * kk) ^ (ln & 7);
-      s8v a[4], b[4];
-#pragma unroll
-      for (int mi = 0; mi < 4; ++mi) a[mi] = As[(64 * wr + 16 * mi + ln) * 8 + sl];
-#pragma unroll
-      for (int ni = 0; ni < 4; ++ni) b[ni] = Bs[(64 * wc + 16 * ni + ln) * 8 + sl];
-#pragma unroll
-      for (int mi = 0; mi < 4; ++mi)
-#pragma unroll
-        for (int ni = 0; ni < 4; ++ni) acc[mi][ni] = mfma16(a[mi], b[ni], acc[mi][ni]);
-    }
-  }
-  const bool vdiv = (ga.vT != nullptr) && (z == 0) && (n0 >= 1536) && (n0 < 2304);
-  const int om = ga.outMode[z];
-#pragma unroll
-  for (int ni = 0; ni < 4; ++ni) {
-    const int n = n0 + 64 * wc + 16 * ni + ln;
-    const float bv = ga.bias[z] ? ga.bias[z][n] : 0.f;
-#pragma unroll
-    for (int mi = 0; mi < 4; ++mi) {
-      const int mb = m0 + 64 * wr + 16 * mi + 4 * lq;
-      if (vdiv) {
-        U4 o4;
-#pragma unroll
-        for (int r = 0; r < 4; ++r) o4.h[r] = __float2bfloat16(acc[mi][ni][r] + bv);
-        *(uint2*)(ga.vT + (size_t)(n - 1536) * S + mb) = o4.u;
-      } else if (om == 0) {
-        bf16* C = (bf16*)ga.C[z];
-#pragma unroll
-        for (int r = 0; r < 4; ++r)
-          C[(size_t)(mb + r) * N + n] = __float2bfloat16(acc[mi][ni][r] + bv);
-      } else {
-        float* C = (float*)ga.C[z];
-#pragma unroll
-        for (int r = 0; r < 4; ++r)
-          C[(size_t)(mb + r) * N + n] = sigmoidf_(acc[mi][ni][r] + bv);
-      }
-    }
-  }
-}
-
-struct GemmPairArgs {
-  const bf16* A0[2]; int lda0[2];
-  const bf16* A1[2]; int lda1[2];
-  const bf16* Bt[2];
-  const float* bias[2];
-  bf16* C[2];
-  int K[2]; int amode[2];
-};
-
-DEV s8v combineRT(s8v x, s8v y, int amode) {
-  U8 ux, uy, r;
-  ux.s = x; uy.s = y;
-#pragma unroll
-  for (int j = 0; j < 8; ++j) {
-    const float fx = __bfloat162float(ux.h[j]);
-    const float fy = __bfloat162float(uy.h[j]);
-    const float tt = sigmoidf_(fx);
-    r.h[j] = __float2bfloat16((amode == 2 ? fx * tt : tt) * fy);
-  }
-  return r.s;
-}
-
-__global__ __launch_bounds__(256) void gemm_pair(GemmPairArgs ga, int N) {
-  __shared__ s8v As[128 * 8];
-  __shared__ s8v Bs[128 * 8];
-  const int z = blockIdx.z;
-  const bf16* A0 = ga.A0[z]; const int lda0 = ga.lda0[z];
-  const bf16* A1 = ga.A1[z]; const int lda1 = ga.lda1[z];
-  const bf16* Bt = ga.Bt[z];
-  const float* bias = ga.bias[z];
-  bf16* C = ga.C[z];
-  const int K = ga.K[z], amode = ga.amode[z];
-  const int t = threadIdx.x;
-  const int lane = t & 63, wid = t >> 6;
-  const int wr = wid >> 1, wc = wid & 1;
-  const int ln = lane & 15, lq = lane >> 4;
-  const int m0 = blockIdx.y * 128, n0 = blockIdx.x * 128;
-  int rowS[4], slS[4], swz[4];
-#pragma unroll
-  for (int q = 0; q < 4; ++q) {
-    const int u = q * 256 + t;
-    rowS[q] = u >> 3; slS[q] = u & 7;
-    swz[q] = rowS[q] * 8 + (slS[q] ^ (rowS[q] & 7));
-  }
-  f4v acc[4][4] = {};
-  s8v ra[4], ra2[4], rb[4];
-#pragma unroll
-  for (int q = 0; q < 4; ++q) {
-    ra[q] = *(const s8v*)(A0 + (size_t)(m0 + rowS[q]) * lda0 + slS[q] * 8);
-    if (amode != 0) ra2[q] = *(const s8v*)(A1 + (size_t)(m0 + rowS[q]) * lda1 + slS[q] * 8);
-    rb[q] = *(const s8v*)(Bt + (size_t)(n0 + rowS[q]) * K + slS[q] * 8);
-  }
-  for (int ks = 0;;) {
-    __syncthreads();
-#pragma unroll
-    for (int q = 0; q < 4; ++q) {
-      As[swz[q]] = (amode == 0) ? ra[q] : combineRT(ra[q], ra2[q], amode);
-      Bs[swz[q]] = rb[q];
-    }
-    const int ksn = ks + 64;
-    if (ksn < K) {
-#pragma unroll
-      for (int q = 0; q < 4; ++q) {
-        ra[q] = *(const s8v*)(A0 + (size_t)(m0 + rowS[q]) * lda0 + ksn + slS[q] * 8);
-        if (amode != 0) ra2[q] = *(const s8v*)(A1 + (size_t)(m0 + rowS[q]) * lda1 + ksn + slS[q] * 8);
-        rb[q] = *(const s8v*)(Bt + (size_t)(n0 + rowS[q]) * K + ksn + slS[q] * 8);
-      }
-    }
-    __syncthreads();
-#pragma unroll
-    for (int kk = 0; kk < 2; ++kk) {
-      const int sl = (lq + 4 * kk) ^ (ln & 7);
-      s8v a[4], b[4];
-#pragma unroll
-      for (int mi = 0; mi < 4; ++mi) a[mi] = As[(64 * wr + 16 * mi + ln) * 8 + sl];
-#pragma unroll
-      for (int ni = 0; ni < 4; ++ni) b[ni] = Bs[(64 * wc + 16 * ni + ln) * 8 + sl];
-#pragma unroll
-      for (int mi = 0; mi < 4; ++mi)
-#pragma unroll
-        for (int ni = 0; ni < 4; ++ni) acc[mi][ni] = mfma16(a[mi], b[ni], acc[mi][ni]);
-    }
-    ks = ksn;
-    if (ks >= K) break;
-  }
-#pragma unroll
-  for (int ni = 0; ni < 4; ++ni) {
-    const int n = n0 + 64 * wc + 16 * ni + ln;
-    const float bv = bias ? bias[n] : 0.f;
-#pragma unroll
-    for (int mi = 0; mi < 4; ++mi) {
-      const int mb = m0 + 64 * wr + 16 * mi + 4 * lq;
-#pragma unroll
-      for (int r = 0; r < 4; ++r)
-        C[(size_t)(mb + r) * N + n] = __float2bfloat16(acc[mi][ni][r] + bv);
-    }
-  }
-}
-
-__global__ __launch_bounds__(256) void flash_attn(const bf16* __restrict__ qkvg,
-                                                  const bf16* __restrict__ vT,
-                                                  const bf16* __restrict__ bias_all,
-                                                  bf16* __restrict__ ob, int blk) {
-  __shared__ s8v Qs[64 * 8];
-  __shared__ s8v Ks[2][64 * 8];
-  __shared__ s8v Vs[2][48 * 8];
-  __shared__ s8v Bs[2][64 * 8];
-  __shared__ bf16 PwB[4 * 1024];
-  __shared__ float facL[4][16];
-  __shared__ float linvL[4][16];
-  const int t = threadIdx.x;
-  const int lane = t & 63, w = t >> 6;
-  const int ln = lane & 15, lq = lane >> 4;
-  const int h = blockIdx.y, i0 = blockIdx.x * 64;
-  const bf16* bp = bias_all + (size_t)(blk * NHEAD + h) * S * S;
-  const float scale = 0.14433756729740643f;
-
-#pragma unroll
-  for (int uu = 0; uu < 2; ++uu) {
-    const int u = t + 256 * uu, row = u >> 3, sl = u & 7;
-    s8v qv{};
-    if (sl < 6) qv = *(const s8v*)(qkvg + (size_t)(i0 + row) * 3072 + h * DH + sl * 8);
-    Qs[row * 8 + (sl ^ (row & 7))] = qv;
-  }
-
-  s8v kr[2], br[2], vr0{}, vr1{};
-  auto prefetch = [&](int jt) {
-    const int j0 = jt * 64;
-#pragma unroll
-    for (int uu = 0; uu < 2; ++uu) {
-      const int u = t + 256 * uu, row = u >> 3, sl = u & 7;
-      s8v kv{};
-      if (sl < 6) kv = *(const s8v*)(qkvg + (size_t)(j0 + row) * 3072 + 768 + h * DH + sl * 8);
-      kr[uu] = kv;
-      br[uu] = *(const s8v*)(bp + (size_t)(i0 + row) * S + j0 + sl * 8);
-    }
-    { const int d = t >> 3, sl = t & 7;
-      vr0 = *(const s8v*)(vT + (size_t)(h * DH + d) * S + j0 + sl * 8); }
-    if (t < 128) {
-      const int u = 256 + t, d = u >> 3, sl = u & 7;
-      vr1 = *(const s8v*)(vT + (size_t)(h * DH + d) * S + j0 + sl * 8);
-    }
-  };
-  auto store_tiles = [&](int pb) {
-#pragma unroll
-    for (int uu = 0; uu < 2; ++uu) {
-      const int u = t + 256 * uu, row = u >> 3, sl = u & 7;
-      const int ph = row * 8 + (sl ^ (row & 7));
-      Ks[pb][ph] = kr[uu];
-      Bs[pb][ph] = br[uu];
-    }
-    { const int d = t >> 3, sl = t & 7;
-      Vs[pb][d * 8 + (sl ^ (d & 7))] = vr0; }
-    if (t < 128) {
-      const int u = 256 + t, d = u >> 3, sl = u & 7;
-      Vs[pb][d * 8 + (sl ^ (d & 7))] = vr1;
-    }
-  };
-
-  float m_run = -3e30f, l_run = 0.f;
-  f4v acc_o[3] = {};
-  bf16* pw = PwB + w * 1024;
-
-  prefetch(0);
-  for (int jt = 0; jt < 16; ++jt) {
-    const int pb = jt & 1;
-    __syncthreads();
-    store_tiles(pb);
-    __syncthreads();
-    if (jt < 15) prefetch(jt + 1);
-    float p[4][4];
-    float tmax = -3e30f;
-#pragma unroll
-    for (int ja = 0; ja < 4; ++ja) {
-      f4v accs = {};
-#pragma unroll
-      for (int ks2 = 0; ks2 < 2; ++ks2) {
-        const int sl = (lq + 4 * ks2) ^ (ln & 7);
-        const s8v a = Ks[pb][(16 * ja + ln) * 8 + sl];
-        const s8v b = Qs[(16 * w + ln) * 8 + sl];
-        accs = mfma16(a, b, accs);
-      }
-      const int jq = 4 * ja + lq;
-      const int pu = jq >> 1;
-      U4 bv;
-      bv.u = *(const uint2*)((const bf16*)(&Bs[pb][0]) +
-                             (((16 * w + ln) * 8 + (pu ^ (ln & 7))) * 8 + (jq & 1) * 4));
-#pragma unroll
-      for (int r = 0; r < 4; ++r) {
-        p[ja][r] = accs[r] * scale + __bfloat162float(bv.h[r]);
-        tmax = fmaxf(tmax, p[ja][r]);
-      }
-    }
-    tmax = fmaxf(tmax, __shfl_xor(tmax, 16));
-    tmax = fmaxf(tmax, __shfl_xor(tmax, 32));
-    const float m_new = fmaxf(m_run, tmax);
-    const float fac = __expf(m_run - m_new);
-    m_run = m_new;
-    float psum = 0.f;
-#pragma unroll
-    for (int ja = 0; ja < 4; ++ja)
-#pragma unroll
-      for (int r = 0; r < 4; ++r) {
-        p[ja][r] = __expf(p[ja][r] - m_new);
-        psum += p[ja][r];
-      }
-    psum += __shfl_xor(psum, 16);
-    psum += __shfl_xor(psum, 32);
-    l_run = l_run * fac + psum;
-    if (lq == 0) facL[w][ln] = fac;
-#pragma unroll
-    for (int ja = 0; ja < 4; ++ja) {
-      const int ju = 4 * ja + lq;
-      const int ph = ju ^ ((ln & 7) << 1);
-      U4 pk;
-#pragma unroll
-      for (int r = 0; r < 4; ++r) pk.h[r] = __float2bfloat16(p[ja][r]);
-      *(uint2*)(pw + ln * 64 + ph * 4) = pk.u;
-    }
-    asm volatile("s_waitcnt lgkmcnt(0)" ::: "memory");
-    __builtin_amdgcn_sched_barrier(0);
-    const float4 fv = *(const float4*)&facL[w][4 * lq];
-#pragma unroll
-    for (int ni = 0; ni < 3; ++ni) {
-      acc_o[ni][0] *= fv.x; acc_o[ni][1] *= fv.y;
-      acc_o[ni][2] *= fv.z; acc_o[ni][3] *= fv.w;
-    }
-#pragma unroll
-    for (int ks2 = 0; ks2 < 2; ++ks2) {
-      const int pu0 = (2 * lq + 8 * ks2) ^ ((ln & 7) << 1);
-      const s8v pa = *(const s8v*)(pw + ln * 64 + pu0 * 4);
-      const int slv = (lq + 4 * ks2) ^ (ln & 7);
-#pragma unroll
-      for (int ni = 0; ni < 3; ++ni) {
-        const s8v vb = Vs[pb][(16 * ni + ln) * 8 + slv];
-        acc_o[ni] = mfma16(pa, vb, acc_o[ni]);
-      }
-    }
-  }
-  if (lq == 0) linvL[w][ln] = 1.0f / l_run;
-  asm volatile("s_waitcnt lgkmcnt(0)" ::: "memory");
-  __builtin_amdgcn_sched_barrier(0);
-  const float4 lv = *(const float4*)&linvL[w][4 * lq];
-  const float lvr[4] = {lv.x, lv.y, lv.z, lv.w};
-#pragma unroll
-  for (int ni = 0; ni < 3; ++ni)
-#pragma unroll
-    for (int r = 0; r < 4; ++r) {
-      const int m = i0 + 16 * w + 4 * lq + r;
-      ob[(size_t)m * CA + h * DH + 16 * ni + ln] = __float2bfloat16(acc_o[ni][r] * lvr[r]);
-    }
 }
 
 __global__ __launch_bounds__(256) void ew_final(const float* __restrict__ sg,
@@ -730,51 +766,35 @@
 
   const dim3 B256(256);
 
-  prep_all<<<49, B256, 0, stream>>>(ln_z_w, ln_z_b, wpb, W2T, bias2,
-                                    bq, bsg_attn, bsg_tr, biasQKVG, biasSG);
-
   {
-    TGroup g{};
-    g.src[0] = wg_attn;  g.dst[0] = WT_ada + (size_t)0 * 384;    g.cs[0] = ln_s_w_attn; g.dstZ[0] = 3072 * 384;
-    g.src[1] = wb_attn;  g.dst[1] = WT_ada + (size_t)768 * 384;  g.cs[1] = ln_s_w_attn; g.dstZ[1] = 3072 * 384;
-    g.src[2] = wg_tr;    g.dst[2] = WT_ada + (size_t)1536 * 384; g.cs[2] = ln_s_w_tr;   g.dstZ[2] = 3072 * 384;
-    g.src[3] = wb_tr;    g.dst[3] = WT_ada + (size_t)2304 * 384; g.cs[3] = ln_s_w_tr;   g.dstZ[3] = 3072 * 384;
-    g.src[4] = wsg_attn; g.dst[4] = WT_sg + (size_t)0 * 384;     g.cs[4] = nullptr;     g.dstZ[4] = 1536 * 384;
-    g.src[5] = wsg_tr;   g.dst[5] = WT_sg + (size_t)768 * 384;   g.cs[5] = nullptr;     g.dstZ[5] = 1536 * 384;
-    transpose_grp<<<dim3(24, 12, 24), B256, 0, stream>>>(g, 384, 768, CS);
-  }
+    PrepFatArgs pa{};
+    pa.tsrc[0] = wg_attn;  pa.tdst[0] = WT_ada + (size_t)0 * 384;    pa.tcs[0] = ln_s_w_attn; pa.tdstZ[0] = 3072 * 384;
+    pa.tsrc[1] = wb_attn;  pa.tdst[1] = WT_ada + (size_t)768 * 384;  pa.tcs[1] = ln_s_w_attn; pa.tdstZ[1] = 3072 * 384;
+    pa.tsrc[2] = wg_tr;    pa.tdst[2] = WT_ada + (size_t)1536 * 384; pa.tcs[2] = ln_s_w_tr;   pa.tdstZ[2] = 3072 * 384;
+    pa.tsrc[3] = wb_tr;    pa.tdst[3] = WT_ada + (size_t)2304 * 384; pa.tcs[3] = ln_s_w_tr;   pa.tdstZ[3] = 3072 * 384;
+    pa.tsrc[4] = wsg_attn; pa.tdst[4] = WT_sg + (size_t)0 * 384;     pa.tcs[4] = nullptr;     pa.tdstZ[4] = 1536 * 384;
+    pa.tsrc[5] = wsg_tr;   pa.tdst[5] = WT_sg + (size_t)768 * 384;   pa.tcs[5] = nullptr;     pa.tdstZ[5] = 1536 * 384;
+    pa.tsrc[6] = wq;    pa.tdst[6] = WT_qkvg + (size_t)0 * 768;    pa.tdstZ[6] = 3072 * 768;
+    pa.tsrc[7] = wk;    pa.tdst[7] = WT_qkvg + (size_t)768 * 768;  pa.tdstZ[7] = 3072 * 768;
+    pa.tsrc[8] = wv;    pa.tdst[8] = WT_qkvg + (size_t)1536 * 768; pa.tdstZ[8] = 3072 * 768;
+    pa.tsrc[9] = wgate; pa.tdst[9] = WT_qkvg + (size_t)2304 * 768; pa.tdstZ[9] = 3072 * 768;
+    pa.tsrc[10] = wo;   pa.tdst[10] = WT_wo;                       pa.tdstZ[10] = 768 * 768;
+    pa.tsrc[11] = w_swish; pa.tdst[11] = WT_mlp + (size_t)0 * 768;    pa.tdstZ[11] = 3072 * 768;
+    pa.tsrc[12] = w_gate2; pa.tdst[12] = WT_mlp + (size_t)1536 * 768; pa.tdstZ[12] = 3072 * 768;
+    pa.tsrc[13] = w_out; pa.tdst[13] = WT_wout; pa.tdstZ[13] = 768 * 1536;
+    pa.ln_z_w = ln_z_w; pa.ln_z_b = ln_z_b; pa.wpb = wpb;
+    pa.bq = bq; pa.bsg_a = bsg_attn; pa.bsg_t = bsg_tr;
+    pa.W2T = W2T; pa.bias2 = bias2; pa.biasQKVG = biasQKVG; pa.biasSG = biasSG;
+    pa.s_in = s_in; pa.s_hat = s_hat; pa.s_bf = s_bf;
+    prep_fat<<<33329, B256, 0, stream>>>(pa);
+  }
+
   {
-    TGroup g{};
-    g.src[0] = wq;    g.dst[0] = WT_qkvg + (size_t)0 * 768;    g.dstZ[0] = 3072 * 768;
-    g.src[1] = wk;    g.dst[1] = WT_qkvg + (size_t)768 * 768;  g.dstZ[1] = 3072 * 768;
-    g.src[2] = wv;    g.dst[2] = WT_qkvg + (size_t)1536 * 768; g.dstZ[2] = 3072 * 768;
-    g.src[3] = wgate; g.dst[3] = WT_qkvg + (size_t)2304 * 768; g.dstZ[3] = 3072 * 768;
-    g.src[4] = wo;    g.dst[4] = WT_wo;                        g.dstZ[4] = 768 * 768;
-    transpose_grp<<<dim3(24, 24, 20), B256, 0, stream>>>(g, 768, 768, 0);
-  }
-  {
-    TGroup g{};
-    g.src[0] = w_swish; g.dst[0] = WT_mlp + (size_t)0 * 768;    g.dstZ[0] = 3072 * 768;
-    g.src[1] = w_gate2; g.dst[1] = WT_mlp + (size_t)1536 * 768; g.dstZ[1] = 3072 * 768;
-    transpose_grp<<<dim3(48, 24, 8), B256, 0, stream>>>(g, 768, 1536, 0);
-  }
-  {
-    TGroup g{};
-    g.src[0] = w_out; g.dst[0] = WT_wout; g.dstZ[0] = 768 * 1536;
-    transpose_grp<<<dim3(24, 48, 4), B256, 0, stream>>>(g, 1536, 768, 0);
-  }
-
-  rowln_s<<<S, B256, 0, stream>>>(s_in, s_hat, s_bf);
-  zbias_kernel<<<dim3(16, 1024), B256, 0, stream>>>(z_in, beta, W2T, bias2, bias_all);
-
-  {
-    Gemm2Args ga{};
-    ga.A0[0] = s_hat; ga.lda0[0] = 384; ga.Bt[0] = WT_ada; ga.bias[0] = nullptr;
-    ga.C[0] = ada_all; ga.K[0] = 384; ga.nb[0] = 96; ga.outMode[0] = 0; ga.N[0] = 12288;
-    ga.A0[1] = s_bf; ga.lda0[1] = 384; ga.Bt[1] = WT_sg; ga.bias[1] = biasSG;
-    ga.C[1] = sg_all; ga.K[1] = 384; ga.nb[1] = 48; ga.outMode[1] = 1; ga.N[1] = 6144;
-    ga.vT = nullptr;
-    gemm2<<<dim3(96, 8, 2), B256, 0, stream>>>(ga);
+    Mega1Args ma{};
+    ma.z = z_in; ma.beta = beta; ma.W2T = W2T; ma.bias2 = bias2; ma.bias_all = bias_all;
+    ma.s_hat = s_hat; ma.s_bf = s_bf; ma.WT_ada = WT_ada; ma.WT_sg = WT_sg;
+    ma.biasSG = biasSG; ma.ada_all = ada_all; ma.sg_all = sg_all;
+    mega1<<<17536, B256, 0, stream>>>(ma);
   }
 
   ln_adaln2<<<S, B256, 0, stream>>>(a_in, ada_all, ah_attn, ah_tr);
@@ -782,25 +802,19 @@
     {
       Gemm2Args ga{};
       ga.A0[0] = ah_attn; ga.lda0[0] = 768; ga.Bt[0] = WT_qkvg + (size_t)b * 3072 * 768;
-      ga.bias[0] = biasQKVG + b * 3072; ga.C[0] = qkvg; ga.K[0] = 768; ga.nb[0] = 24;
-      ga.outMode[0] = 0; ga.N[0] = 3072;
+      ga.bias[0] = biasQKVG + b * 3072; ga.C[0] = qkvg; ga.K[0] = 768; ga.N[0] = 3072;
       ga.A0[1] = ah_tr; ga.lda0[1] = 768; ga.Bt[1] = WT_mlp + (size_t)b * 3072 * 768;
-      ga.bias[1] = nullptr; ga.C[1] = swg; ga.K[1] = 768; ga.nb[1] = 24;
-      ga.outMode[1] = 0; ga.N[1] = 3072;
+      ga.bias[1] = nullptr; ga.C[1] = swg; ga.K[1] = 768; ga.N[1] = 3072;
       ga.vT = vT;
       gemm2<<<dim3(24, 8, 2), B256, 0, stream>>>(ga);
     }
-    flash_attn<<<dim3(16, 16), B256, 0, stream>>>(qkvg, vT, bias_all, ob, b);
     {
-      GemmPairArgs ga{};
-      ga.A0[0] = qkvg + 2304; ga.lda0[0] = 3072; ga.A1[0] = ob; ga.lda1[0] = 768;
-      ga.Bt[0] = WT_wo + (size_t)b * 768 * 768; ga.bias[0] = nullptr;
-      ga.C[0] = att; ga.K[0] = 768; ga.amode[0] = 1;
-      ga.A0[1] = swg; ga.lda0[1] = 3072; ga.A1[1] = swg + 1536; ga.lda1[1] = 3072;
-      ga.Bt[1] = WT_wout + (size_t)b * 768 * 1536; ga.bias[1] = nullptr;
-      ga.C[1] = trout; ga.K[1] = 1536; ga.amode[1] = 2;
-      gemm_pair<<<dim3(6, 8, 2), B256, 0, stream>>>(ga, 768);
-    }
+      FlashFatArgs fa{};
+      fa.qkvg = qkvg; fa.vT = vT; fa.bias_b = bias_all + (size_t)b * NHEAD * S * S; fa.ob = ob;
+      fa.swg = swg; fa.WT_wout_b = WT_wout + (size_t)b * 768 * 1536; fa.trout = trout;
+      flash_fat<<<304, B256, 0, stream>>>(fa);
+    }
+    gemm_wo<<<dim3(6, 8), B256, 0, stream>>>(qkvg + 2304, ob, WT_wo + (size_t)b * 768 * 768, att);
     if (b < NBLK - 1) {
       final_adaln<<<S, B256, 0, stream>>>(sg_all + (size_t)b * 1536, att, trout,
                                           ada_all + (size_t)(b + 1) * 3072, ah_attn, ah_tr);
```

Result: no change. 689.6 us (+1.9%).
